# Kernel tuning notes

Measured on AMD Instinct MI355X. Metric: run time of the kernel, lower is better.

The kernel has to match this reference:

```python
import jax, jax.numpy as jnp
import numpy as np

D_INP = 36
D_MODEL = 144              # 4*d_inp so d_ob == 4 (required by increase_dim view: d_ob*8 == 32)
D_OB = D_MODEL // D_INP    # 4
D_PE = 16
MAX_LEN = 215
NHEAD = 4
NHID = 256
NLAYERS = 2
B = 8
L = MAX_LEN
C = MAX_LEN * D_OB         # 860: ob-propagation node feature width
E = D_INP * D_INP          # dense sensor graph incl. self loops
K = E // 2                 # edges kept after pruning (use_beta path)
D_TR = D_MODEL + D_PE      # 160: transformer width


def _layernorm(x, w, b, eps=1e-5):
    mu = x.mean(-1, keepdims=True)
    var = ((x - mu) ** 2).mean(-1, keepdims=True)
    return (x - mu) * jax.lax.rsqrt(var + eps) * w + b


def _pos_encode(times):
    # times [L,B] -> sinusoidal PE [L,B,16] (PositionalEncodingTF)
    ts = jnp.asarray(MAX_LEN ** np.linspace(0.0, 1.0, D_PE // 2), jnp.float32)
    scaled = times[..., None] / ts
    return jnp.concatenate([jnp.sin(scaled), jnp.cos(scaled)], axis=-1)


def _graph_prop(x, p_t, src, dst, ew, W_inc, b_inc, map_w):
    # Two stacked Observation_progation layers for ONE sample.
    # x [N,C] sensor features, p_t [L,16], edges src->dst, edge weights ew [E].
    x_i = x[dst]                                            # target node feats per edge
    x_j = x[src]                                            # source node feats per edge
    hW = (x_i @ W_inc.T + b_inc).reshape(E, L, 32)          # increase_dim + view
    # beta = mean(h_W * cat([map_w[dst] bcast, p_t bcast], -1), -1), computed without materializing aa
    beta = (jnp.einsum('ets,es->et', hW[..., :D_PE], map_w[dst]) +
            jnp.einsum('ets,ts->et', hW[..., D_PE:], p_t)) / 32.0
    gamma = jnp.repeat(beta * ew[:, None], D_OB, axis=-1)   # [E,C]
    top = jnp.argsort(-gamma.mean(axis=1))[:K]              # prune half of the edges
    gamma_p = gamma[top]
    src_p = src[top]
    dst_p = dst[top]
    alpha = gamma_p.mean(axis=-1)                           # layer-1 attention weights [K]
    msg1 = jax.nn.relu(x_j[top]) * jax.nn.relu(gamma_p)
    h1 = jax.ops.segment_sum(msg1, dst_p, num_segments=D_INP)
    # layer 2: use_beta=False, edge_weights = alpha, same pruned edge set
    msg2 = jax.nn.relu(h1[src_p]) * jax.nn.relu(alpha)[:, None]
    h2 = jax.ops.segment_sum(msg2, dst_p, num_segments=D_INP)
    return h2, alpha


def _encoder_layer(x, pad_mask, qkv_w, qkv_b, out_w, out_b,
                   ff1_w, ff1_b, ff2_w, ff2_b, ln1_w, ln1_b, ln2_w, ln2_b):
    # torch post-norm TransformerEncoderLayer (relu, eval mode); x [B,L,D]
    Bq, Lq, D = x.shape
    dh = D // NHEAD
    q, k, v = jnp.split(x @ qkv_w.T + qkv_b, 3, axis=-1)
    hd = lambda t: t.reshape(Bq, Lq, NHEAD, dh).transpose(0, 2, 1, 3)
    scores = jnp.einsum('bhqd,bhkd->bhqk', hd(q), hd(k)) / jnp.sqrt(jnp.float32(dh))
    scores = jnp.where(pad_mask[:, None, None, :], -1e9, scores)  # src_key_padding_mask
    ctx = jnp.einsum('bhqk,bhkd->bhqd', jax.nn.softmax(scores, axis=-1), hd(v))
    ctx = ctx.transpose(0, 2, 1, 3).reshape(Bq, Lq, D)
    x = _layernorm(x + ctx @ out_w.T + out_b, ln1_w, ln1_b)
    ff = jax.nn.relu(x @ ff1_w.T + ff1_b) @ ff2_w.T + ff2_b
    return _layernorm(x + ff, ln2_w, ln2_b)


def _forward(event_type, event_time, R_u, global_structure,
             ob1_W_inc, ob1_b_inc, ob1_map_w, layer_params, w_time, w_type):
    non_pad = (event_type != 0).astype(jnp.float32)[..., None]      # [B,L,1]
    lengths = non_pad[..., 0].sum(axis=-1).astype(jnp.int32)        # [B]
    times = event_time.T                                            # [L,B]
    idx = jnp.maximum(event_type - 1, 0)
    src = jax.nn.one_hot(idx, D_INP, dtype=jnp.float32)             # [B,L,N]
    src = jnp.repeat(jnp.transpose(src, (1, 0, 2)), D_OB, axis=-1)  # [L,B,N*d_ob]
    h = jax.nn.relu(src * R_u[0])                                   # relu(src * R_u)
    pe = _pos_encode(times)                                         # [L,B,16]
    pad_mask = jnp.arange(L)[None, :] >= lengths[:, None]           # [B,L]

    eye = jnp.eye(D_INP, dtype=jnp.float32)
    adj = global_structure * (1.0 - eye) + eye                      # diagonal set to 1
    src_e = jnp.repeat(jnp.arange(D_INP), D_INP)                    # edge_index[0] (row-major nonzero)
    dst_e = jnp.tile(jnp.arange(D_INP), D_INP)                      # edge_index[1]
    ew = adj.reshape(-1)

    def per_sample(xu, pu):  # xu [L,144], pu [L,16]
        sd = xu.reshape(L, D_INP, D_OB).transpose(1, 0, 2).reshape(D_INP, C)
        h2, alpha = _graph_prop(sd, pu, src_e, dst_e, ew, ob1_W_inc, ob1_b_inc, ob1_map_w)
        return h2.reshape(D_INP, L, D_OB).transpose(1, 0, 2).reshape(L, D_INP * D_OB), alpha

    gout, alpha_all = jax.vmap(per_sample, in_axes=(1, 1), out_axes=(1, 1))(h, pe)
    A = alpha_all.T                                                 # [B,K]
    d2 = jnp.sum((A[:, None, :] - A[None, :, :]) ** 2, axis=-1)
    distance = jnp.mean(jnp.where(d2 > 0, jnp.sqrt(jnp.where(d2 > 0, d2, 1.0)), 0.0))

    x = jnp.transpose(jnp.concatenate([gout, pe], axis=2), (1, 0, 2))  # [B,L,160]
    for p in layer_params:
        x = _encoder_layer(x, pad_mask, *p)
    output = x                                                      # == transpose(r_out, 0, 1)
    time_pred = (output @ w_time.T) * non_pad
    type_pred = (output @ w_type.T) * non_pad
    return output, type_pred, time_pred, distance


def setup_inputs():
    key = jax.random.key(0)
    kit = iter(jax.random.split(key, 40))
    def nrm(shape, s=0.05):
        return jax.random.normal(next(kit), shape, dtype=jnp.float32) * s
    lengths = jax.random.randint(next(kit), (B,), 100, L + 1)
    et = jax.random.randint(next(kit), (B, L), 1, D_INP + 1)
    pad = jnp.arange(L)[None, :] >= lengths[:, None]
    inp = {
        'event_type': jnp.where(pad, 0, et).astype(jnp.int32),
        'event_time': jnp.cumsum(jax.random.uniform(next(kit), (B, L)), axis=1).astype(jnp.float32),
        'R_u': nrm((1, D_INP * D_OB), 0.2),
        'global_structure': jax.random.uniform(next(kit), (D_INP, D_INP), minval=0.5, maxval=1.5, dtype=jnp.float32),
        'ob1_W_inc': nrm((C * 8, C), 0.02),
        'ob1_b_inc': jnp.zeros((C * 8,), jnp.float32),
        'ob1_map_w': nrm((D_INP, D_PE), 0.2),
        'w_time': nrm((1, D_TR)),
        'w_type': nrm((D_INP, D_TR)),
    }
    for i in range(NLAYERS):
        inp[f'l{i}_qkv_w'] = nrm((3 * D_TR, D_TR))
        inp[f'l{i}_qkv_b'] = jnp.zeros((3 * D_TR,), jnp.float32)
        inp[f'l{i}_out_w'] = nrm((D_TR, D_TR))
        inp[f'l{i}_out_b'] = jnp.zeros((D_TR,), jnp.float32)
        inp[f'l{i}_ff1_w'] = nrm((NHID, D_TR))
        inp[f'l{i}_ff1_b'] = jnp.zeros((NHID,), jnp.float32)
        inp[f'l{i}_ff2_w'] = nrm((D_TR, NHID))
        inp[f'l{i}_ff2_b'] = jnp.zeros((D_TR,), jnp.float32)
        inp[f'l{i}_ln1_w'] = jnp.ones((D_TR,), jnp.float32)
        inp[f'l{i}_ln1_b'] = jnp.zeros((D_TR,), jnp.float32)
        inp[f'l{i}_ln2_w'] = jnp.ones((D_TR,), jnp.float32)
        inp[f'l{i}_ln2_b'] = jnp.zeros((D_TR,), jnp.float32)
    return inp


def reference(event_type, event_time, R_u, global_structure, ob1_W_inc, ob1_b_inc, ob1_map_w,
              l0_qkv_w, l0_qkv_b, l0_out_w, l0_out_b, l0_ff1_w, l0_ff1_b, l0_ff2_w, l0_ff2_b,
              l0_ln1_w, l0_ln1_b, l0_ln2_w, l0_ln2_b,
              l1_qkv_w, l1_qkv_b, l1_out_w, l1_out_b, l1_ff1_w, l1_ff1_b, l1_ff2_w, l1_ff2_b,
              l1_ln1_w, l1_ln1_b, l1_ln2_w, l1_ln2_b, w_time, w_type):
    lp = [
        (l0_qkv_w, l0_qkv_b, l0_out_w, l0_out_b, l0_ff1_w, l0_ff1_b, l0_ff2_w, l0_ff2_b,
         l0_ln1_w, l0_ln1_b, l0_ln2_w, l0_ln2_b),
        (l1_qkv_w, l1_qkv_b, l1_out_w, l1_out_b, l1_ff1_w, l1_ff1_b, l1_ff2_w, l1_ff2_b,
         l1_ln1_w, l1_ln1_b, l1_ln2_w, l1_ln2_b),
    ]
    return _forward(event_type, event_time, R_u, global_structure,
                    ob1_W_inc, ob1_b_inc, ob1_map_w, lp, w_time, w_type)
```

## Files before the change

kernel.cpp:

```cpp
#include <hip/hip_runtime.h>
#include <math.h>

#define NBATCH 8
#define LMAX   215
#define NND    36
#define NE     1296
#define NK     648
#define CW     860
#define DPE    16
#define DTR    160
#define NHEADS 4
#define DH     40
#define NHID2  256
#define NPAIR  (NBATCH*LMAX)
#define KSPLIT 8
#define KQLEN  27
#define ROWS   4

#define OUT_TYPE (NBATCH*LMAX*DTR)
#define OUT_TIME (OUT_TYPE + NBATCH*LMAX*NND)
#define OUT_DIST (OUT_TIME + NBATCH*LMAX)

#define OFF_PE    0
#define OFF_RR    (OFF_PE + NBATCH*LMAX*DPE)
#define OFF_EW    (OFF_RR + 144)
#define OFF_BETA  (OFF_EW + NE)
#define OFF_ALPHA (OFF_BETA + NBATCH*NND*LMAX)
#define OFF_H1    (OFF_ALPHA + NBATCH*NK)
#define OFF_X     (OFF_H1 + NBATCH*NND*CW)
#define OFF_X2    (OFF_X + NBATCH*LMAX*DTR)
#define OFF_QKV   (OFF_X2 + NBATCH*LMAX*DTR)
#define OFF_TOPI  (OFF_QKV + NBATCH*LMAX*480)
#define OFF_IDX   (OFF_TOPI + NBATCH*NK)
#define OFF_LENS  (OFF_IDX + NBATCH*LMAX)
#define OFF_PART  (OFF_LENS + NBATCH)
#define OFF_CSRC  (OFF_PART + 32*KSPLIT*LMAX*42)
#define OFF_CSRL  (OFF_CSRC + NBATCH*NND)
#define OFF_WT    (OFF_CSRL + NBATCH*NND*LMAX)

__global__ __launch_bounds__(256) void k_wt(
        const float* __restrict__ q0, const float* __restrict__ o0,
        const float* __restrict__ f10, const float* __restrict__ f20,
        const float* __restrict__ q1, const float* __restrict__ o1,
        const float* __restrict__ f11, const float* __restrict__ f21,
        float* __restrict__ wt) {
    int mat = blockIdx.y;
    const float* src; float* dst; int R, C;
    switch (mat) {
        case 0: src = q0;  dst = wt + 0;               R = 480; C = DTR;   break;
        case 1: src = o0;  dst = wt + 76800;           R = DTR; C = DTR;   break;
        case 2: src = f10; dst = wt + 102400;          R = NHID2; C = DTR; break;
        case 3: src = f20; dst = wt + 143360;          R = DTR; C = NHID2; break;
        case 4: src = q1;  dst = wt + 184320;          R = 480; C = DTR;   break;
        case 5: src = o1;  dst = wt + 184320 + 76800;  R = DTR; C = DTR;   break;
        case 6: src = f11; dst = wt + 184320 + 102400; R = NHID2; C = DTR; break;
        default: src = f21; dst = wt + 184320 + 143360; R = DTR; C = NHID2; break;
    }
    int total = R * C;
    for (int i = blockIdx.x * 256 + threadIdx.x; i < total; i += gridDim.x * 256) {
        int r = i / C, c = i - r * C;
        dst[c * R + r] = src[i];
    }
}

__global__ __launch_bounds__(256) void k_prep(
        const int* __restrict__ et, const float* __restrict__ etime,
        const float* __restrict__ Ru, const float* __restrict__ gs,
        float* pe, float* rr, float* ew, int* idxarr, int* lens,
        int* csr_cnt, int* csr_list, float* __restrict__ x) {
    int blk = blockIdx.x, tid = threadIdx.x;
    if (blk == 0) {
        for (int c = tid; c < 144; c += 256) rr[c] = fmaxf(Ru[c], 0.f);
        for (int e = tid; e < NE; e += 256) {
            int r = e / NND, cc = e % NND;
            ew[e] = (r == cc) ? 1.0f : gs[e];
        }
    } else if (blk <= 8) {
        int b = blk - 1;
        __shared__ int red[256];
        __shared__ int sidx[LMAX];
        int cnt = 0;
        for (int l = tid; l < LMAX; l += 256) {
            int v = et[b * LMAX + l];
            cnt += (v != 0);
            int ix = max(v - 1, 0);
            idxarr[b * LMAX + l] = ix;
            sidx[l] = ix;
        }
        red[tid] = cnt;
        __syncthreads();
        for (int st = 128; st > 0; st >>= 1) { if (tid < st) red[tid] += red[tid + st]; __syncthreads(); }
        if (tid == 0) lens[b] = red[0];
        if (tid < NND) {
            int c = 0;
            int* lst = csr_list + (size_t)(b * NND + tid) * LMAX;
            for (int l = 0; l < LMAX; ++l)
                if (sidx[l] == tid) { lst[c] = l; ++c; }
            csr_cnt[b * NND + tid] = c;
        }
    } else {
        __shared__ float sts[8];
        if (tid < 8) sts[tid] = (float)pow(215.0, (double)tid / 7.0);
        __syncthreads();
        int i0 = (blk - 9) * 430;
        for (int i = i0 + tid; i < i0 + 430; i += 256) {
            int s = i & 15; int bl = i >> 4;
            float t = etime[bl];
            float sc = t / sts[s & 7];
            float v = (s < 8) ? sinf(sc) : cosf(sc);
            pe[i] = v;
            x[(size_t)bl * DTR + 144 + s] = v;
        }
    }
}

__global__ __launch_bounds__(256) void k_beta(
        const float* __restrict__ Winc, const float* __restrict__ binc,
        const float* __restrict__ mapw, const float* __restrict__ pe,
        const float* __restrict__ rr, const int* __restrict__ idxarr,
        const int* __restrict__ csr_cnt, const int* __restrict__ csr_list,
        float* __restrict__ beta) {
    const int t = blockIdx.x;
    const int tid = threadIdx.x;

    __shared__ float s_rows[2][4 * CW];
    __shared__ float s_pair[NBATCH * LMAX];
    __shared__ int   s_idx[NPAIR];
    __shared__ float s_mapw[NND * 16];
    __shared__ float s_rr[144];
    __shared__ float s_pe[NBATCH * 16];
    __shared__ float s_binc[32];

    for (int i = tid; i < NPAIR; i += 256) s_idx[i] = idxarr[i];
    for (int i = tid; i < NND * 16; i += 256) s_mapw[i] = mapw[i];
    if (tid < 144) s_rr[tid] = rr[tid];
    if (tid < 128) { int b = tid >> 4, s = tid & 15; s_pe[tid] = pe[((size_t)(b * LMAX + t)) * DPE + s]; }
    if (tid < 32) s_binc[tid] = binc[32 * t + tid];

    float4 pre[4];
    {
        const float4* src = (const float4*)(Winc + (size_t)(32 * t) * CW);
#pragma unroll
        for (int i = 0; i < 4; ++i) { int k = tid + i * 256; if (k < CW) pre[i] = src[k]; }
    }
    __syncthreads();

    const int l = tid;
    int nb[NBATCH];
    float4 r4b[NBATCH];
    if (l < LMAX) {
#pragma unroll
        for (int b = 0; b < NBATCH; ++b) {
            nb[b] = s_idx[b * LMAX + l];
            r4b[b] = *(const float4*)&s_rr[4 * nb[b]];
        }
    }
    float acc[NBATCH];
#pragma unroll
    for (int b = 0; b < NBATCH; ++b) acc[b] = 0.f;

    int p = 0;
    for (int jc = 0; jc < 8; ++jc) {
        float4* buf = (float4*)&s_rows[p][0];
#pragma unroll
        for (int i = 0; i < 4; ++i) { int k = tid + i * 256; if (k < CW) buf[k] = pre[i]; }
        __syncthreads();
        if (jc < 7) {
            const float4* src = (const float4*)(Winc + (size_t)(32 * t + 4 * (jc + 1)) * CW);
#pragma unroll
            for (int i = 0; i < 4; ++i) { int k = tid + i * 256; if (k < CW) pre[i] = src[k]; }
        }
        if (l < LMAX) {
            if (jc < 4) {
#pragma unroll
                for (int jj = 0; jj < 4; ++jj) {
                    int j = 4 * jc + jj;
                    float4 w4 = *(const float4*)&s_rows[p][jj * CW + 4 * l];
#pragma unroll
                    for (int b = 0; b < NBATCH; ++b) {
                        float dv = r4b[b].x * w4.x + r4b[b].y * w4.y + r4b[b].z * w4.z + r4b[b].w * w4.w;
                        acc[b] += s_mapw[nb[b] * 16 + j] * dv;
                    }
                }
            } else {
#pragma unroll
                for (int jj = 0; jj < 4; ++jj) {
                    int j = 4 * jc + jj;
                    float4 w4 = *(const float4*)&s_rows[p][jj * CW + 4 * l];
#pragma unroll
                    for (int b = 0; b < NBATCH; ++b) {
                        float dv = r4b[b].x * w4.x + r4b[b].y * w4.y + r4b[b].z * w4.z + r4b[b].w * w4.w;
                        acc[b] += s_pe[(b << 4) + (j - 16)] * dv;
                    }
                }
            }
        }
        __syncthreads();
        p ^= 1;
    }

    if (l < LMAX) {
#pragma unroll
        for (int b = 0; b < NBATCH; ++b) s_pair[b * LMAX + l] = acc[b];
    }
    __syncthreads();

    for (int bn = tid; bn < NBATCH * NND; bn += 256) {
        int b = bn / NND, n = bn - b * NND;
        int cnt = csr_cnt[bn];
        const int* lst = csr_list + (size_t)bn * LMAX;
        float sum = 0.f;
        for (int i = 0; i < cnt; ++i) sum += s_pair[b * LMAX + lst[i]];
        float bias = 0.f;
#pragma unroll
        for (int s = 0; s < 16; ++s)
            bias += s_mapw[n * 16 + s] * s_binc[s] + s_pe[(b << 4) + s] * s_binc[16 + s];
        beta[(size_t)bn * LMAX + t] = (sum + bias) * (1.0f / 32.0f);
    }
}

__global__ __launch_bounds__(256) void k_topk(const float* __restrict__ ew,
                                              const float* __restrict__ beta,
                                              int* __restrict__ topi, float* __restrict__ alpha) {
    int chunk = blockIdx.x;
    int b = blockIdx.y;
    int tid = threadIdx.x;
    __shared__ float sv[NE];
    __shared__ float sm[NND];
    int wv = tid >> 6, lane = tid & 63;
    for (int n = wv; n < NND; n += 4) {
        const float* p = beta + (size_t)(b * NND + n) * LMAX;
        float s = 0.f;
        for (int t = lane; t < LMAX; t += 64) s += p[t];
        for (int off = 32; off > 0; off >>= 1) s += __shfl_xor(s, off);
        if (lane == 0) sm[n] = s / (float)LMAX;
    }
    __syncthreads();
    for (int e = tid; e < NE; e += 256) sv[e] = ew[e] * sm[e % NND];
    __syncthreads();
    int e = chunk * 216 + tid;
    if (tid < 216) {
        float v = sv[e];
        int rank = 0;
        for (int i = 0; i < NE; ++i) {
            float u = sv[i];
            rank += (u > v) || (u == v && i < e);
        }
        if (rank < NK) {
            topi[b * NK + rank] = e;
            alpha[b * NK + rank] = v;
        }
    }
}

__global__ void k_h1(const int* __restrict__ topi, const float* __restrict__ ew,
                     const float* __restrict__ beta, const int* __restrict__ idxarr,
                     const float* __restrict__ rr, const float* __restrict__ alpha,
                     float* h1, float* __restrict__ outd) {
    int b = blockIdx.x / NND, n = blockIdx.x % NND;
    __shared__ int cnt;
    __shared__ int lsrc[40];
    __shared__ float lew[40];
    int tid = threadIdx.x;
    if (tid == 0) cnt = 0;
    __syncthreads();
    for (int k = tid; k < NK; k += 256) {
        int e = topi[b * NK + k];
        if (e % NND == n) {
            int p = atomicAdd(&cnt, 1);
            lsrc[p] = e / NND;
            lew[p] = ew[e];
        }
    }
    __syncthreads();
    int m = cnt;
    const float* bb = beta + ((size_t)b * NND + n) * LMAX;
    for (int c = tid; c < CW; c += 256) {
        int t = c >> 2, o = c & 3;
        float bt = bb[t];
        int id = idxarr[b * LMAX + t];
        float x = rr[id * 4 + o];
        float acc = 0.f;
        for (int j = 0; j < m; ++j) {
            float g = bt * lew[j];
            if (g > 0.f && lsrc[j] == id) acc += x * g;
        }
        h1[((size_t)b * NND + n) * CW + c] = acc;
    }
    if (blockIdx.x == 0) {
        __shared__ float sd[64];
        if (tid < 64) {
            int i = tid / 8, j = tid % 8;
            float d2 = 0.f;
            for (int k = 0; k < NK; ++k) {
                float d = alpha[i * NK + k] - alpha[j * NK + k];
                d2 += d * d;
            }
            sd[tid] = (d2 > 0.f) ? sqrtf(d2) : 0.f;
        }
        __syncthreads();
        for (int st = 32; st > 0; st >>= 1) { if (tid < st) sd[tid] += sd[tid + st]; __syncthreads(); }
        if (tid == 0) *outd = sd[0] / 64.0f;
    }
}

__global__ void k_h2(const int* __restrict__ topi, const float* __restrict__ alpha,
                     const float* __restrict__ h1, float* __restrict__ x) {
    int b = blockIdx.x / NND, n = blockIdx.x % NND;
    __shared__ int cnt;
    __shared__ int lsrc[40];
    __shared__ float lal[40];
    int tid = threadIdx.x;
    if (tid == 0) cnt = 0;
    __syncthreads();
    for (int k = tid; k < NK; k += 256) {
        int e = topi[b * NK + k];
        if (e % NND == n) {
            int p = atomicAdd(&cnt, 1);
            lsrc[p] = e / NND;
            lal[p] = fmaxf(alpha[b * NK + k], 0.f);
        }
    }
    __syncthreads();
    int m = cnt;
    for (int c = tid; c < CW; c += 256) {
        float acc = 0.f;
        for (int j = 0; j < m; ++j)
            acc += fmaxf(h1[((size_t)b * NND + lsrc[j]) * CW + c], 0.f) * lal[j];
        x[(size_t)(b * LMAX + (c >> 2)) * DTR + 4 * n + (c & 3)] = acc;
    }
}

__global__ __launch_bounds__(256) void k_qkv(const float* __restrict__ X, const float* __restrict__ WT,
                                             const float* __restrict__ bias, float* __restrict__ Y) {
    int m0 = blockIdx.x * ROWS;
    int tid = threadIdx.x;
    __shared__ float xs[ROWS * DTR];
    for (int i = tid; i < ROWS * DTR; i += 256) xs[i] = X[(size_t)m0 * DTR + i];
    __syncthreads();
    for (int n = tid; n < 480; n += 256) {
        float a[ROWS][4];
#pragma unroll
        for (int r = 0; r < ROWS; ++r) { a[r][0] = a[r][1] = a[r][2] = a[r][3] = 0.f; }
        for (int d = 0; d < DTR; d += 4) {
            float w0 = WT[(size_t)(d + 0) * 480 + n];
            float w1 = WT[(size_t)(d + 1) * 480 + n];
            float w2 = WT[(size_t)(d + 2) * 480 + n];
            float w3 = WT[(size_t)(d + 3) * 480 + n];
#pragma unroll
            for (int r = 0; r < ROWS; ++r) {
                a[r][0] += xs[r * DTR + d] * w0;
                a[r][1] += xs[r * DTR + d + 1] * w1;
                a[r][2] += xs[r * DTR + d + 2] * w2;
                a[r][3] += xs[r * DTR + d + 3] * w3;
            }
        }
        float bv = bias[n];
#pragma unroll
        for (int r = 0; r < ROWS; ++r)
            Y[(size_t)(m0 + r) * 480 + n] = bv + (a[r][0] + a[r][1]) + (a[r][2] + a[r][3]);
    }
}

__global__ __launch_bounds__(256) void k_attn_part(const float* __restrict__ qkv,
                                                   const int* __restrict__ lens,
                                                   float* __restrict__ part) {
    int kq = blockIdx.x;
    int bh = blockIdx.y;
    int b = bh >> 2, h = bh & 3;
    int tid = threadIdx.x;
    int k0 = kq * KQLEN;
    int k1 = min(LMAX, k0 + KQLEN);
    int klen = max(k1 - k0, 0);
    __shared__ float sK[KQLEN * DH];
    __shared__ float sV[KQLEN * DH];
    for (int i = tid; i < klen * DH; i += 256) {
        int kk = i / DH, d = i - kk * DH;
        size_t base = (size_t)(b * LMAX + k0 + kk) * 480;
        sK[i] = qkv[base + DTR + h * DH + d];
        sV[i] = qkv[base + 2 * DTR + h * DH + d];
    }
    __syncthreads();
    int q = tid;
    if (q >= LMAX) return;
    float4 qv[10];
    const float4* qr = (const float4*)(qkv + (size_t)(b * LMAX + q) * 480 + h * DH);
#pragma unroll
    for (int i = 0; i < 10; ++i) qv[i] = qr[i];
    int len = lens[b];
    const float scale = 0.15811388300841898f;
    float m = -INFINITY, l = 0.f;
    float o[DH];
#pragma unroll
    for (int d = 0; d < DH; ++d) o[d] = 0.f;
    int kend = min(k1, len);
    for (int k = k0; k < kend; ++k) {
        const float4* kr = (const float4*)&sK[(k - k0) * DH];
        float s0 = 0.f, s1 = 0.f, s2 = 0.f, s3 = 0.f;
#pragma unroll
        for (int i = 0; i < 10; ++i) {
            float4 kv = kr[i];
            s0 += qv[i].x * kv.x; s1 += qv[i].y * kv.y;
            s2 += qv[i].z * kv.z; s3 += qv[i].w * kv.w;
        }
        float s = ((s0 + s1) + (s2 + s3)) * scale;
        float p;
        if (s <= m) {
            p = expf(s - m);
        } else {
            float c = expf(m - s);
#pragma unroll
            for (int d = 0; d < DH; ++d) o[d] *= c;
            l *= c;
            m = s;
            p = 1.0f;
        }
        l += p;
        const float* vr = &sV[(k - k0) * DH];
#pragma unroll
        for (int d = 0; d < DH; ++d) o[d] += p * vr[d];
    }
    float* pp = part + ((size_t)(bh * KSPLIT + kq) * LMAX + q) * 42;
#pragma unroll
    for (int d = 0; d < DH; ++d) pp[d] = o[d];
    pp[40] = l;
    pp[41] = m;
}

__device__ __forceinline__ void wave_ln_row(const float* __restrict__ row, int lane,
                                            const float* __restrict__ lnw, const float* __restrict__ lnb,
                                            float* __restrict__ dst) {
    float s = 0.f;
    for (int d = lane; d < DTR; d += 64) s += row[d];
    for (int off = 32; off > 0; off >>= 1) s += __shfl_xor(s, off);
    float mu = s / (float)DTR;
    float v = 0.f;
    for (int d = lane; d < DTR; d += 64) { float dd = row[d] - mu; v += dd * dd; }
    for (int off = 32; off > 0; off >>= 1) v += __shfl_xor(v, off);
    float rs = rsqrtf(v / (float)DTR + 1e-5f);
    for (int d = lane; d < DTR; d += 64)
        dst[d] = (row[d] - mu) * rs * lnw[d] + lnb[d];
}

__global__ __launch_bounds__(256) void k_projln(const float* __restrict__ part, const float* __restrict__ xres,
                                                const float* __restrict__ WT, const float* __restrict__ bias,
                                                const float* __restrict__ lnw, const float* __restrict__ lnb,
                                                float* __restrict__ out) {
    int m0 = blockIdx.x * ROWS;
    int tid = threadIdx.x;
    __shared__ float xs[ROWS * DTR];
    __shared__ float ys[ROWS * DTR];
    int g = tid >> 6, lane = tid & 63;
    for (int pr = g; pr < ROWS * NHEADS; pr += 4) {
        int r = pr >> 2, h = pr & 3;
        int row = m0 + r;
        int b = row / LMAX, q = row - b * LMAX;
        const float* pb = part + ((size_t)((b * NHEADS + h) * KSPLIT) * LMAX + q) * 42;
        const size_t st = (size_t)LMAX * 42;
        float ms = -INFINITY;
#pragma unroll
        for (int i = 0; i < KSPLIT; ++i) ms = fmaxf(ms, pb[i * st + 41]);
        float lsum = 0.f, acc = 0.f;
#pragma unroll
        for (int i = 0; i < KSPLIT; ++i) {
            float w = expf(pb[i * st + 41] - ms);
            lsum += w * pb[i * st + 40];
            if (lane < DH) acc += w * pb[i * st + lane];
        }
        if (lane < DH) xs[r * DTR + h * DH + lane] = acc / lsum;
    }
    __syncthreads();
    if (tid < DTR) {
        int n = tid;
        float a[ROWS][4];
#pragma unroll
        for (int r = 0; r < ROWS; ++r) { a[r][0] = a[r][1] = a[r][2] = a[r][3] = 0.f; }
        for (int d = 0; d < DTR; d += 4) {
            float w0 = WT[(size_t)(d + 0) * DTR + n];
            float w1 = WT[(size_t)(d + 1) * DTR + n];
            float w2 = WT[(size_t)(d + 2) * DTR + n];
            float w3 = WT[(size_t)(d + 3) * DTR + n];
#pragma unroll
            for (int r = 0; r < ROWS; ++r) {
                a[r][0] += xs[r * DTR + d] * w0;
                a[r][1] += xs[r * DTR + d + 1] * w1;
                a[r][2] += xs[r * DTR + d + 2] * w2;
                a[r][3] += xs[r * DTR + d + 3] * w3;
            }
        }
        float bv = bias[n];
#pragma unroll
        for (int r = 0; r < ROWS; ++r)
            ys[r * DTR + n] = bv + (a[r][0] + a[r][1]) + (a[r][2] + a[r][3])
                              + xres[(size_t)(m0 + r) * DTR + n];
    }
    __syncthreads();
    if (g < ROWS)
        wave_ln_row(&ys[g * DTR], lane, lnw, lnb, out + (size_t)(m0 + g) * DTR);
}

__global__ __launch_bounds__(256) void k_ffln(const float* __restrict__ xin,
                                              const float* __restrict__ W1T, const float* __restrict__ b1,
                                              const float* __restrict__ W2T, const float* __restrict__ b2,
                                              const float* __restrict__ lnw, const float* __restrict__ lnb,
                                              float* __restrict__ out, int last,
                                              const float* __restrict__ wty, const float* __restrict__ wti,
                                              const int* __restrict__ lens) {
    int m0 = blockIdx.x * ROWS;
    int tid = threadIdx.x;
    __shared__ float xs[ROWS * DTR];
    __shared__ float hs[ROWS * NHID2];
    __shared__ float zs[ROWS * DTR];
    __shared__ float fin[ROWS * DTR];
    for (int i = tid; i < ROWS * DTR; i += 256) xs[i] = xin[(size_t)m0 * DTR + i];
    __syncthreads();
    {
        int n = tid;
        float a[ROWS][4];
#pragma unroll
        for (int r = 0; r < ROWS; ++r) { a[r][0] = a[r][1] = a[r][2] = a[r][3] = 0.f; }
        for (int d = 0; d < DTR; d += 4) {
            float w0 = W1T[(size_t)(d + 0) * NHID2 + n];
            float w1 = W1T[(size_t)(d + 1) * NHID2 + n];
            float w2 = W1T[(size_t)(d + 2) * NHID2 + n];
            float w3 = W1T[(size_t)(d + 3) * NHID2 + n];
#pragma unroll
            for (int r = 0; r < ROWS; ++r) {
                a[r][0] += xs[r * DTR + d] * w0;
                a[r][1] += xs[r * DTR + d + 1] * w1;
                a[r][2] += xs[r * DTR + d + 2] * w2;
                a[r][3] += xs[r * DTR + d + 3] * w3;
            }
        }
        float bv = b1[n];
#pragma unroll
        for (int r = 0; r < ROWS; ++r)
            hs[r * NHID2 + n] = fmaxf(bv + (a[r][0] + a[r][1]) + (a[r][2] + a[r][3]), 0.f);
    }
    __syncthreads();
    if (tid < DTR) {
        int n = tid;
        float a[ROWS][4];
#pragma unroll
        for (int r = 0; r < ROWS; ++r) { a[r][0] = a[r][1] = a[r][2] = a[r][3] = 0.f; }
        for (int d = 0; d < NHID2; d += 4) {
            float w0 = W2T[(size_t)(d + 0) * DTR + n];
            float w1 = W2T[(size_t)(d + 1) * DTR + n];
            float w2 = W2T[(size_t)(d + 2) * DTR + n];
            float w3 = W2T[(size_t)(d + 3) * DTR + n];
#pragma unroll
            for (int r = 0; r < ROWS; ++r) {
                a[r][0] += hs[r * NHID2 + d] * w0;
                a[r][1] += hs[r * NHID2 + d + 1] * w1;
                a[r][2] += hs[r * NHID2 + d + 2] * w2;
                a[r][3] += hs[r * NHID2 + d + 3] * w3;
            }
        }
        float bv = b2[n];
#pragma unroll
        for (int r = 0; r < ROWS; ++r)
            zs[r * DTR + n] = bv + (a[r][0] + a[r][1]) + (a[r][2] + a[r][3]) + xs[r * DTR + n];
    }
    __syncthreads();
    int wid = tid >> 6, lane = tid & 63;
    if (!last) {
        if (wid < ROWS)
            wave_ln_row(&zs[wid * DTR], lane, lnw, lnb, out + (size_t)(m0 + wid) * DTR);
        return;
    }
    if (wid < ROWS)
        wave_ln_row(&zs[wid * DTR], lane, lnw, lnb, &fin[wid * DTR]);
    __syncthreads();
    for (int i = tid; i < ROWS * DTR; i += 256) out[(size_t)m0 * DTR + i] = fin[i];
    {
        int row = m0 + wid;
        int b = row / LMAX, l = row - b * LMAX;
        float np = (l < lens[b]) ? 1.f : 0.f;
        if (lane < 37) {
            const float* w = (lane < 36) ? (wty + lane * DTR) : wti;
            const float* fr = &fin[wid * DTR];
            float acc = 0.f;
#pragma unroll 8
            for (int d = 0; d < DTR; d += 4) {
                float4 w4 = *(const float4*)(w + d);
                acc += fr[d] * w4.x + fr[d + 1] * w4.y + fr[d + 2] * w4.z + fr[d + 3] * w4.w;
            }
            acc *= np;
            if (lane < 36) out[OUT_TYPE + (size_t)row * NND + lane] = acc;
            else out[OUT_TIME + row] = acc;
        }
    }
}

extern "C" void kernel_launch(void* const* d_in, const int* in_sizes, int n_in,
                              void* d_out, int out_size, void* d_ws, size_t ws_size,
                              hipStream_t stream) {
    const int* et      = (const int*)d_in[0];
    const float* etime = (const float*)d_in[1];
    const float* Ru    = (const float*)d_in[2];
    const float* gs    = (const float*)d_in[3];
    const float* Winc  = (const float*)d_in[4];
    const float* binc  = (const float*)d_in[5];
    const float* mapw  = (const float*)d_in[6];
    const float* wtime = (const float*)d_in[7];
    const float* wtype = (const float*)d_in[8];

    float* ws   = (float*)d_ws;
    float* pe   = ws + OFF_PE;
    float* rr   = ws + OFF_RR;
    float* ew   = ws + OFF_EW;
    float* beta = ws + OFF_BETA;
    float* alpha= ws + OFF_ALPHA;
    float* h1   = ws + OFF_H1;
    float* x    = ws + OFF_X;
    float* x2   = ws + OFF_X2;
    float* qkvb = ws + OFF_QKV;
    float* part = ws + OFF_PART;
    float* wt   = ws + OFF_WT;
    int* topi   = (int*)(ws + OFF_TOPI);
    int* idxarr = (int*)(ws + OFF_IDX);
    int* lens   = (int*)(ws + OFF_LENS);
    int* csrc   = (int*)(ws + OFF_CSRC);
    int* csrl   = (int*)(ws + OFF_CSRL);
    float* outp = (float*)d_out;

    k_wt<<<dim3(32, 8), 256, 0, stream>>>(
        (const float*)d_in[9],  (const float*)d_in[11], (const float*)d_in[13], (const float*)d_in[15],
        (const float*)d_in[21], (const float*)d_in[23], (const float*)d_in[25], (const float*)d_in[27], wt);
    k_prep<<<73, 256, 0, stream>>>(et, etime, Ru, gs, pe, rr, ew, idxarr, lens, csrc, csrl, x);
    k_beta<<<LMAX, 256, 0, stream>>>(Winc, binc, mapw, pe, rr, idxarr, csrc, csrl, beta);
    k_topk<<<dim3(6, NBATCH), 256, 0, stream>>>(ew, beta, topi, alpha);
    k_h1<<<NBATCH * NND, 256, 0, stream>>>(topi, ew, beta, idxarr, rr, alpha, h1, outp + OUT_DIST);
    k_h2<<<NBATCH * NND, 256, 0, stream>>>(topi, alpha, h1, x);

    const int MB4 = NPAIR / ROWS;
    for (int layer = 0; layer < 2; ++layer) {
        int base = 9 + layer * 12;
        const float* qkv_b = (const float*)d_in[base + 1];
        const float* out_b = (const float*)d_in[base + 3];
        const float* ff1_b = (const float*)d_in[base + 5];
        const float* ff2_b = (const float*)d_in[base + 7];
        const float* ln1_w = (const float*)d_in[base + 8];
        const float* ln1_b = (const float*)d_in[base + 9];
        const float* ln2_w = (const float*)d_in[base + 10];
        const float* ln2_b = (const float*)d_in[base + 11];
        const float* qkvT = wt + (size_t)layer * 184320;
        const float* outT = qkvT + 76800;
        const float* ff1T = qkvT + 102400;
        const float* ff2T = qkvT + 143360;

        k_qkv<<<MB4, 256, 0, stream>>>(x, qkvT, qkv_b, qkvb);
        k_attn_part<<<dim3(KSPLIT, NBATCH * NHEADS), 256, 0, stream>>>(qkvb, lens, part);
        k_projln<<<MB4, 256, 0, stream>>>(part, x, outT, out_b, ln1_w, ln1_b, x2);
        if (layer == 0)
            k_ffln<<<MB4, 256, 0, stream>>>(x2, ff1T, ff1_b, ff2T, ff2_b, ln2_w, ln2_b,
                                            x, 0, wtype, wtime, lens);
        else
            k_ffln<<<MB4, 256, 0, stream>>>(x2, ff1T, ff1_b, ff2T, ff2_b, ln2_w, ln2_b,
                                            outp, 1, wtype, wtime, lens);
    }
}
```

Baseline: 419.3 us.

## Fuse all stages into one persistent megakernel with software grid barriers

Result: slower. 750.5 us (+79.0%).

```diff
diff --git a/kernel.cpp b/kernel.cpp
--- a/kernel.cpp
+++ b/kernel.cpp
@@ -16,6 +16,8 @@
 #define KSPLIT 8
 #define KQLEN  27
 #define ROWS   4
+#define NBLK   430
+#define MAGIC  0x5A5A5A5A
 
 #define OUT_TYPE (NBATCH*LMAX*DTR)
 #define OUT_TIME (OUT_TYPE + NBATCH*LMAX*NND)
@@ -37,399 +39,49 @@
 #define OFF_CSRC  (OFF_PART + 32*KSPLIT*LMAX*42)
 #define OFF_CSRL  (OFF_CSRC + NBATCH*NND)
 #define OFF_WT    (OFF_CSRL + NBATCH*NND*LMAX)
-
-__global__ __launch_bounds__(256) void k_wt(
-        const float* __restrict__ q0, const float* __restrict__ o0,
-        const float* __restrict__ f10, const float* __restrict__ f20,
-        const float* __restrict__ q1, const float* __restrict__ o1,
-        const float* __restrict__ f11, const float* __restrict__ f21,
-        float* __restrict__ wt) {
-    int mat = blockIdx.y;
-    const float* src; float* dst; int R, C;
-    switch (mat) {
-        case 0: src = q0;  dst = wt + 0;               R = 480; C = DTR;   break;
-        case 1: src = o0;  dst = wt + 76800;           R = DTR; C = DTR;   break;
-        case 2: src = f10; dst = wt + 102400;          R = NHID2; C = DTR; break;
-        case 3: src = f20; dst = wt + 143360;          R = DTR; C = NHID2; break;
-        case 4: src = q1;  dst = wt + 184320;          R = 480; C = DTR;   break;
-        case 5: src = o1;  dst = wt + 184320 + 76800;  R = DTR; C = DTR;   break;
-        case 6: src = f11; dst = wt + 184320 + 102400; R = NHID2; C = DTR; break;
-        default: src = f21; dst = wt + 184320 + 143360; R = DTR; C = NHID2; break;
-    }
-    int total = R * C;
-    for (int i = blockIdx.x * 256 + threadIdx.x; i < total; i += gridDim.x * 256) {
-        int r = i / C, c = i - r * C;
-        dst[c * R + r] = src[i];
-    }
+#define OFF_BAR   (OFF_WT + 2*184320)
+
+struct MegaArgs {
+    const int* et; const float* etime; const float* Ru; const float* gs;
+    const float* Winc; const float* binc; const float* mapw;
+    const float* wtime; const float* wtype;
+    const float* qw[2];  const float* qb[2];
+    const float* ow[2];  const float* ob[2];
+    const float* f1w[2]; const float* f1b[2];
+    const float* f2w[2]; const float* f2b[2];
+    const float* l1w[2]; const float* l1b[2];
+    const float* l2w[2]; const float* l2b[2];
+    float* ws; float* outp;
+};
+
+struct SBeta { float rows[2][4*CW]; float pair[NPAIR]; int idx[NPAIR];
+               float mapw[NND*16]; float rr[144]; float pe[NBATCH*16]; float binc[32]; };
+struct SPrep { int red[256]; int sidx[LMAX]; float sts[8]; };
+struct STopk { float sv[NE]; float sm[NND]; };
+struct SAttn { float K[KQLEN*DH]; float V[KQLEN*DH]; };
+struct SH1   { int cnt; int lsrc[40]; float lew[40]; float sd[64]; };
+struct SH2   { int cnt; int lsrc[40]; float lal[40]; };
+struct SQkv  { float xs[ROWS*DTR]; };
+struct SProj { float xs[ROWS*DTR]; float ys[ROWS*DTR]; };
+struct SFf   { float xs[ROWS*DTR]; float hs[ROWS*NHID2]; float zs[ROWS*DTR]; float fin[ROWS*DTR]; };
+
+__device__ __forceinline__ void gridbar(int* cnt, int* gen, int bi) {
+    __syncthreads();
+    if (threadIdx.x == 0) {
+        int old = __hip_atomic_fetch_add(&cnt[bi], 1, __ATOMIC_ACQ_REL, __HIP_MEMORY_SCOPE_AGENT);
+        if (old == NBLK - 1) {
+            __hip_atomic_store(gen, bi + 1, __ATOMIC_RELEASE, __HIP_MEMORY_SCOPE_AGENT);
+        } else {
+            while (__hip_atomic_load(gen, __ATOMIC_RELAXED, __HIP_MEMORY_SCOPE_AGENT) < bi + 1)
+                __builtin_amdgcn_s_sleep(2);
+            (void)__hip_atomic_load(gen, __ATOMIC_ACQUIRE, __HIP_MEMORY_SCOPE_AGENT);
+        }
+    }
+    __syncthreads();
 }
 
-__global__ __launch_bounds__(256) void k_prep(
-        const int* __restrict__ et, const float* __restrict__ etime,
-        const float* __restrict__ Ru, const float* __restrict__ gs,
-        float* pe, float* rr, float* ew, int* idxarr, int* lens,
-        int* csr_cnt, int* csr_list, float* __restrict__ x) {
-    int blk = blockIdx.x, tid = threadIdx.x;
-    if (blk == 0) {
-        for (int c = tid; c < 144; c += 256) rr[c] = fmaxf(Ru[c], 0.f);
-        for (int e = tid; e < NE; e += 256) {
-            int r = e / NND, cc = e % NND;
-            ew[e] = (r == cc) ? 1.0f : gs[e];
-        }
-    } else if (blk <= 8) {
-        int b = blk - 1;
-        __shared__ int red[256];
-        __shared__ int sidx[LMAX];
-        int cnt = 0;
-        for (int l = tid; l < LMAX; l += 256) {
-            int v = et[b * LMAX + l];
-            cnt += (v != 0);
-            int ix = max(v - 1, 0);
-            idxarr[b * LMAX + l] = ix;
-            sidx[l] = ix;
-        }
-        red[tid] = cnt;
-        __syncthreads();
-        for (int st = 128; st > 0; st >>= 1) { if (tid < st) red[tid] += red[tid + st]; __syncthreads(); }
-        if (tid == 0) lens[b] = red[0];
-        if (tid < NND) {
-            int c = 0;
-            int* lst = csr_list + (size_t)(b * NND + tid) * LMAX;
-            for (int l = 0; l < LMAX; ++l)
-                if (sidx[l] == tid) { lst[c] = l; ++c; }
-            csr_cnt[b * NND + tid] = c;
-        }
-    } else {
-        __shared__ float sts[8];
-        if (tid < 8) sts[tid] = (float)pow(215.0, (double)tid / 7.0);
-        __syncthreads();
-        int i0 = (blk - 9) * 430;
-        for (int i = i0 + tid; i < i0 + 430; i += 256) {
-            int s = i & 15; int bl = i >> 4;
-            float t = etime[bl];
-            float sc = t / sts[s & 7];
-            float v = (s < 8) ? sinf(sc) : cosf(sc);
-            pe[i] = v;
-            x[(size_t)bl * DTR + 144 + s] = v;
-        }
-    }
-}
-
-__global__ __launch_bounds__(256) void k_beta(
-        const float* __restrict__ Winc, const float* __restrict__ binc,
-        const float* __restrict__ mapw, const float* __restrict__ pe,
-        const float* __restrict__ rr, const int* __restrict__ idxarr,
-        const int* __restrict__ csr_cnt, const int* __restrict__ csr_list,
-        float* __restrict__ beta) {
-    const int t = blockIdx.x;
-    const int tid = threadIdx.x;
-
-    __shared__ float s_rows[2][4 * CW];
-    __shared__ float s_pair[NBATCH * LMAX];
-    __shared__ int   s_idx[NPAIR];
-    __shared__ float s_mapw[NND * 16];
-    __shared__ float s_rr[144];
-    __shared__ float s_pe[NBATCH * 16];
-    __shared__ float s_binc[32];
-
-    for (int i = tid; i < NPAIR; i += 256) s_idx[i] = idxarr[i];
-    for (int i = tid; i < NND * 16; i += 256) s_mapw[i] = mapw[i];
-    if (tid < 144) s_rr[tid] = rr[tid];
-    if (tid < 128) { int b = tid >> 4, s = tid & 15; s_pe[tid] = pe[((size_t)(b * LMAX + t)) * DPE + s]; }
-    if (tid < 32) s_binc[tid] = binc[32 * t + tid];
-
-    float4 pre[4];
-    {
-        const float4* src = (const float4*)(Winc + (size_t)(32 * t) * CW);
-#pragma unroll
-        for (int i = 0; i < 4; ++i) { int k = tid + i * 256; if (k < CW) pre[i] = src[k]; }
-    }
-    __syncthreads();
-
-    const int l = tid;
-    int nb[NBATCH];
-    float4 r4b[NBATCH];
-    if (l < LMAX) {
-#pragma unroll
-        for (int b = 0; b < NBATCH; ++b) {
-            nb[b] = s_idx[b * LMAX + l];
-            r4b[b] = *(const float4*)&s_rr[4 * nb[b]];
-        }
-    }
-    float acc[NBATCH];
-#pragma unroll
-    for (int b = 0; b < NBATCH; ++b) acc[b] = 0.f;
-
-    int p = 0;
-    for (int jc = 0; jc < 8; ++jc) {
-        float4* buf = (float4*)&s_rows[p][0];
-#pragma unroll
-        for (int i = 0; i < 4; ++i) { int k = tid + i * 256; if (k < CW) buf[k] = pre[i]; }
-        __syncthreads();
-        if (jc < 7) {
-            const float4* src = (const float4*)(Winc + (size_t)(32 * t + 4 * (jc + 1)) * CW);
-#pragma unroll
-            for (int i = 0; i < 4; ++i) { int k = tid + i * 256; if (k < CW) pre[i] = src[k]; }
-        }
-        if (l < LMAX) {
-            if (jc < 4) {
-#pragma unroll
-                for (int jj = 0; jj < 4; ++jj) {
-                    int j = 4 * jc + jj;
-                    float4 w4 = *(const float4*)&s_rows[p][jj * CW + 4 * l];
-#pragma unroll
-                    for (int b = 0; b < NBATCH; ++b) {
-                        float dv = r4b[b].x * w4.x + r4b[b].y * w4.y + r4b[b].z * w4.z + r4b[b].w * w4.w;
-                        acc[b] += s_mapw[nb[b] * 16 + j] * dv;
-                    }
-                }
-            } else {
-#pragma unroll
-                for (int jj = 0; jj < 4; ++jj) {
-                    int j = 4 * jc + jj;
-                    float4 w4 = *(const float4*)&s_rows[p][jj * CW + 4 * l];
-#pragma unroll
-                    for (int b = 0; b < NBATCH; ++b) {
-                        float dv = r4b[b].x * w4.x + r4b[b].y * w4.y + r4b[b].z * w4.z + r4b[b].w * w4.w;
-                        acc[b] += s_pe[(b << 4) + (j - 16)] * dv;
-                    }
-                }
-            }
-        }
-        __syncthreads();
-        p ^= 1;
-    }
-
-    if (l < LMAX) {
-#pragma unroll
-        for (int b = 0; b < NBATCH; ++b) s_pair[b * LMAX + l] = acc[b];
-    }
-    __syncthreads();
-
-    for (int bn = tid; bn < NBATCH * NND; bn += 256) {
-        int b = bn / NND, n = bn - b * NND;
-        int cnt = csr_cnt[bn];
-        const int* lst = csr_list + (size_t)bn * LMAX;
-        float sum = 0.f;
-        for (int i = 0; i < cnt; ++i) sum += s_pair[b * LMAX + lst[i]];
-        float bias = 0.f;
-#pragma unroll
-        for (int s = 0; s < 16; ++s)
-            bias += s_mapw[n * 16 + s] * s_binc[s] + s_pe[(b << 4) + s] * s_binc[16 + s];
-        beta[(size_t)bn * LMAX + t] = (sum + bias) * (1.0f / 32.0f);
-    }
-}
-
-__global__ __launch_bounds__(256) void k_topk(const float* __restrict__ ew,
-                                              const float* __restrict__ beta,
-                                              int* __restrict__ topi, float* __restrict__ alpha) {
-    int chunk = blockIdx.x;
-    int b = blockIdx.y;
-    int tid = threadIdx.x;
-    __shared__ float sv[NE];
-    __shared__ float sm[NND];
-    int wv = tid >> 6, lane = tid & 63;
-    for (int n = wv; n < NND; n += 4) {
-        const float* p = beta + (size_t)(b * NND + n) * LMAX;
-        float s = 0.f;
-        for (int t = lane; t < LMAX; t += 64) s += p[t];
-        for (int off = 32; off > 0; off >>= 1) s += __shfl_xor(s, off);
-        if (lane == 0) sm[n] = s / (float)LMAX;
-    }
-    __syncthreads();
-    for (int e = tid; e < NE; e += 256) sv[e] = ew[e] * sm[e % NND];
-    __syncthreads();
-    int e = chunk * 216 + tid;
-    if (tid < 216) {
-        float v = sv[e];
-        int rank = 0;
-        for (int i = 0; i < NE; ++i) {
-            float u = sv[i];
-            rank += (u > v) || (u == v && i < e);
-        }
-        if (rank < NK) {
-            topi[b * NK + rank] = e;
-            alpha[b * NK + rank] = v;
-        }
-    }
-}
-
-__global__ void k_h1(const int* __restrict__ topi, const float* __restrict__ ew,
-                     const float* __restrict__ beta, const int* __restrict__ idxarr,
-                     const float* __restrict__ rr, const float* __restrict__ alpha,
-                     float* h1, float* __restrict__ outd) {
-    int b = blockIdx.x / NND, n = blockIdx.x % NND;
-    __shared__ int cnt;
-    __shared__ int lsrc[40];
-    __shared__ float lew[40];
-    int tid = threadIdx.x;
-    if (tid == 0) cnt = 0;
-    __syncthreads();
-    for (int k = tid; k < NK; k += 256) {
-        int e = topi[b * NK + k];
-        if (e % NND == n) {
-            int p = atomicAdd(&cnt, 1);
-            lsrc[p] = e / NND;
-            lew[p] = ew[e];
-        }
-    }
-    __syncthreads();
-    int m = cnt;
-    const float* bb = beta + ((size_t)b * NND + n) * LMAX;
-    for (int c = tid; c < CW; c += 256) {
-        int t = c >> 2, o = c & 3;
-        float bt = bb[t];
-        int id = idxarr[b * LMAX + t];
-        float x = rr[id * 4 + o];
-        float acc = 0.f;
-        for (int j = 0; j < m; ++j) {
-            float g = bt * lew[j];
-            if (g > 0.f && lsrc[j] == id) acc += x * g;
-        }
-        h1[((size_t)b * NND + n) * CW + c] = acc;
-    }
-    if (blockIdx.x == 0) {
-        __shared__ float sd[64];
-        if (tid < 64) {
-            int i = tid / 8, j = tid % 8;
-            float d2 = 0.f;
-            for (int k = 0; k < NK; ++k) {
-                float d = alpha[i * NK + k] - alpha[j * NK + k];
-                d2 += d * d;
-            }
-            sd[tid] = (d2 > 0.f) ? sqrtf(d2) : 0.f;
-        }
-        __syncthreads();
-        for (int st = 32; st > 0; st >>= 1) { if (tid < st) sd[tid] += sd[tid + st]; __syncthreads(); }
-        if (tid == 0) *outd = sd[0] / 64.0f;
-    }
-}
-
-__global__ void k_h2(const int* __restrict__ topi, const float* __restrict__ alpha,
-                     const float* __restrict__ h1, float* __restrict__ x) {
-    int b = blockIdx.x / NND, n = blockIdx.x % NND;
-    __shared__ int cnt;
-    __shared__ int lsrc[40];
-    __shared__ float lal[40];
-    int tid = threadIdx.x;
-    if (tid == 0) cnt = 0;
-    __syncthreads();
-    for (int k = tid; k < NK; k += 256) {
-        int e = topi[b * NK + k];
-        if (e % NND == n) {
-            int p = atomicAdd(&cnt, 1);
-            lsrc[p] = e / NND;
-            lal[p] = fmaxf(alpha[b * NK + k], 0.f);
-        }
-    }
-    __syncthreads();
-    int m = cnt;
-    for (int c = tid; c < CW; c += 256) {
-        float acc = 0.f;
-        for (int j = 0; j < m; ++j)
-            acc += fmaxf(h1[((size_t)b * NND + lsrc[j]) * CW + c], 0.f) * lal[j];
-        x[(size_t)(b * LMAX + (c >> 2)) * DTR + 4 * n + (c & 3)] = acc;
-    }
-}
-
-__global__ __launch_bounds__(256) void k_qkv(const float* __restrict__ X, const float* __restrict__ WT,
-                                             const float* __restrict__ bias, float* __restrict__ Y) {
-    int m0 = blockIdx.x * ROWS;
-    int tid = threadIdx.x;
-    __shared__ float xs[ROWS * DTR];
-    for (int i = tid; i < ROWS * DTR; i += 256) xs[i] = X[(size_t)m0 * DTR + i];
-    __syncthreads();
-    for (int n = tid; n < 480; n += 256) {
-        float a[ROWS][4];
-#pragma unroll
-        for (int r = 0; r < ROWS; ++r) { a[r][0] = a[r][1] = a[r][2] = a[r][3] = 0.f; }
-        for (int d = 0; d < DTR; d += 4) {
-            float w0 = WT[(size_t)(d + 0) * 480 + n];
-            float w1 = WT[(size_t)(d + 1) * 480 + n];
-            float w2 = WT[(size_t)(d + 2) * 480 + n];
-            float w3 = WT[(size_t)(d + 3) * 480 + n];
-#pragma unroll
-            for (int r = 0; r < ROWS; ++r) {
-                a[r][0] += xs[r * DTR + d] * w0;
-                a[r][1] += xs[r * DTR + d + 1] * w1;
-                a[r][2] += xs[r * DTR + d + 2] * w2;
-                a[r][3] += xs[r * DTR + d + 3] * w3;
-            }
-        }
-        float bv = bias[n];
-#pragma unroll
-        for (int r = 0; r < ROWS; ++r)
-            Y[(size_t)(m0 + r) * 480 + n] = bv + (a[r][0] + a[r][1]) + (a[r][2] + a[r][3]);
-    }
-}
-
-__global__ __launch_bounds__(256) void k_attn_part(const float* __restrict__ qkv,
-                                                   const int* __restrict__ lens,
-                                                   float* __restrict__ part) {
-    int kq = blockIdx.x;
-    int bh = blockIdx.y;
-    int b = bh >> 2, h = bh & 3;
-    int tid = threadIdx.x;
-    int k0 = kq * KQLEN;
-    int k1 = min(LMAX, k0 + KQLEN);
-    int klen = max(k1 - k0, 0);
-    __shared__ float sK[KQLEN * DH];
-    __shared__ float sV[KQLEN * DH];
-    for (int i = tid; i < klen * DH; i += 256) {
-        int kk = i / DH, d = i - kk * DH;
-        size_t base = (size_t)(b * LMAX + k0 + kk) * 480;
-        sK[i] = qkv[base + DTR + h * DH + d];
-        sV[i] = qkv[base + 2 * DTR + h * DH + d];
-    }
-    __syncthreads();
-    int q = tid;
-    if (q >= LMAX) return;
-    float4 qv[10];
-    const float4* qr = (const float4*)(qkv + (size_t)(b * LMAX + q) * 480 + h * DH);
-#pragma unroll
-    for (int i = 0; i < 10; ++i) qv[i] = qr[i];
-    int len = lens[b];
-    const float scale = 0.15811388300841898f;
-    float m = -INFINITY, l = 0.f;
-    float o[DH];
-#pragma unroll
-    for (int d = 0; d < DH; ++d) o[d] = 0.f;
-    int kend = min(k1, len);
-    for (int k = k0; k < kend; ++k) {
-        const float4* kr = (const float4*)&sK[(k - k0) * DH];
-        float s0 = 0.f, s1 = 0.f, s2 = 0.f, s3 = 0.f;
-#pragma unroll
-        for (int i = 0; i < 10; ++i) {
-            float4 kv = kr[i];
-            s0 += qv[i].x * kv.x; s1 += qv[i].y * kv.y;
-            s2 += qv[i].z * kv.z; s3 += qv[i].w * kv.w;
-        }
-        float s = ((s0 + s1) + (s2 + s3)) * scale;
-        float p;
-        if (s <= m) {
-            p = expf(s - m);
-        } else {
-            float c = expf(m - s);
-#pragma unroll
-            for (int d = 0; d < DH; ++d) o[d] *= c;
-            l *= c;
-            m = s;
-            p = 1.0f;
-        }
-        l += p;
-        const float* vr = &sV[(k - k0) * DH];
-#pragma unroll
-        for (int d = 0; d < DH; ++d) o[d] += p * vr[d];
-    }
-    float* pp = part + ((size_t)(bh * KSPLIT + kq) * LMAX + q) * 42;
-#pragma unroll
-    for (int d = 0; d < DH; ++d) pp[d] = o[d];
-    pp[40] = l;
-    pp[41] = m;
-}
-
-__device__ __forceinline__ void wave_ln_row(const float* __restrict__ row, int lane,
-                                            const float* __restrict__ lnw, const float* __restrict__ lnb,
-                                            float* __restrict__ dst) {
+__device__ __forceinline__ void wave_ln_row(const float* row, int lane,
+                                            const float* lnw, const float* lnb, float* dst) {
     float s = 0.f;
     for (int d = lane; d < DTR; d += 64) s += row[d];
     for (int off = 32; off > 0; off >>= 1) s += __shfl_xor(s, off);
@@ -442,221 +94,570 @@
         dst[d] = (row[d] - mu) * rs * lnw[d] + lnb[d];
 }
 
-__global__ __launch_bounds__(256) void k_projln(const float* __restrict__ part, const float* __restrict__ xres,
-                                                const float* __restrict__ WT, const float* __restrict__ bias,
-                                                const float* __restrict__ lnw, const float* __restrict__ lnb,
-                                                float* __restrict__ out) {
-    int m0 = blockIdx.x * ROWS;
-    int tid = threadIdx.x;
-    __shared__ float xs[ROWS * DTR];
-    __shared__ float ys[ROWS * DTR];
-    int g = tid >> 6, lane = tid & 63;
-    for (int pr = g; pr < ROWS * NHEADS; pr += 4) {
-        int r = pr >> 2, h = pr & 3;
-        int row = m0 + r;
-        int b = row / LMAX, q = row - b * LMAX;
-        const float* pb = part + ((size_t)((b * NHEADS + h) * KSPLIT) * LMAX + q) * 42;
-        const size_t st = (size_t)LMAX * 42;
-        float ms = -INFINITY;
-#pragma unroll
-        for (int i = 0; i < KSPLIT; ++i) ms = fmaxf(ms, pb[i * st + 41]);
-        float lsum = 0.f, acc = 0.f;
-#pragma unroll
-        for (int i = 0; i < KSPLIT; ++i) {
-            float w = expf(pb[i * st + 41] - ms);
-            lsum += w * pb[i * st + 40];
-            if (lane < DH) acc += w * pb[i * st + lane];
-        }
-        if (lane < DH) xs[r * DTR + h * DH + lane] = acc / lsum;
-    }
-    __syncthreads();
-    if (tid < DTR) {
-        int n = tid;
-        float a[ROWS][4];
-#pragma unroll
-        for (int r = 0; r < ROWS; ++r) { a[r][0] = a[r][1] = a[r][2] = a[r][3] = 0.f; }
-        for (int d = 0; d < DTR; d += 4) {
-            float w0 = WT[(size_t)(d + 0) * DTR + n];
-            float w1 = WT[(size_t)(d + 1) * DTR + n];
-            float w2 = WT[(size_t)(d + 2) * DTR + n];
-            float w3 = WT[(size_t)(d + 3) * DTR + n];
-#pragma unroll
-            for (int r = 0; r < ROWS; ++r) {
-                a[r][0] += xs[r * DTR + d] * w0;
-                a[r][1] += xs[r * DTR + d + 1] * w1;
-                a[r][2] += xs[r * DTR + d + 2] * w2;
-                a[r][3] += xs[r * DTR + d + 3] * w3;
-            }
-        }
-        float bv = bias[n];
-#pragma unroll
-        for (int r = 0; r < ROWS; ++r)
-            ys[r * DTR + n] = bv + (a[r][0] + a[r][1]) + (a[r][2] + a[r][3])
-                              + xres[(size_t)(m0 + r) * DTR + n];
-    }
-    __syncthreads();
-    if (g < ROWS)
-        wave_ln_row(&ys[g * DTR], lane, lnw, lnb, out + (size_t)(m0 + g) * DTR);
-}
-
-__global__ __launch_bounds__(256) void k_ffln(const float* __restrict__ xin,
-                                              const float* __restrict__ W1T, const float* __restrict__ b1,
-                                              const float* __restrict__ W2T, const float* __restrict__ b2,
-                                              const float* __restrict__ lnw, const float* __restrict__ lnb,
-                                              float* __restrict__ out, int last,
-                                              const float* __restrict__ wty, const float* __restrict__ wti,
-                                              const int* __restrict__ lens) {
-    int m0 = blockIdx.x * ROWS;
-    int tid = threadIdx.x;
-    __shared__ float xs[ROWS * DTR];
-    __shared__ float hs[ROWS * NHID2];
-    __shared__ float zs[ROWS * DTR];
-    __shared__ float fin[ROWS * DTR];
-    for (int i = tid; i < ROWS * DTR; i += 256) xs[i] = xin[(size_t)m0 * DTR + i];
-    __syncthreads();
-    {
-        int n = tid;
-        float a[ROWS][4];
-#pragma unroll
-        for (int r = 0; r < ROWS; ++r) { a[r][0] = a[r][1] = a[r][2] = a[r][3] = 0.f; }
-        for (int d = 0; d < DTR; d += 4) {
-            float w0 = W1T[(size_t)(d + 0) * NHID2 + n];
-            float w1 = W1T[(size_t)(d + 1) * NHID2 + n];
-            float w2 = W1T[(size_t)(d + 2) * NHID2 + n];
-            float w3 = W1T[(size_t)(d + 3) * NHID2 + n];
-#pragma unroll
-            for (int r = 0; r < ROWS; ++r) {
-                a[r][0] += xs[r * DTR + d] * w0;
-                a[r][1] += xs[r * DTR + d + 1] * w1;
-                a[r][2] += xs[r * DTR + d + 2] * w2;
-                a[r][3] += xs[r * DTR + d + 3] * w3;
-            }
-        }
-        float bv = b1[n];
-#pragma unroll
-        for (int r = 0; r < ROWS; ++r)
-            hs[r * NHID2 + n] = fmaxf(bv + (a[r][0] + a[r][1]) + (a[r][2] + a[r][3]), 0.f);
-    }
-    __syncthreads();
-    if (tid < DTR) {
-        int n = tid;
-        float a[ROWS][4];
-#pragma unroll
-        for (int r = 0; r < ROWS; ++r) { a[r][0] = a[r][1] = a[r][2] = a[r][3] = 0.f; }
-        for (int d = 0; d < NHID2; d += 4) {
-            float w0 = W2T[(size_t)(d + 0) * DTR + n];
-            float w1 = W2T[(size_t)(d + 1) * DTR + n];
-            float w2 = W2T[(size_t)(d + 2) * DTR + n];
-            float w3 = W2T[(size_t)(d + 3) * DTR + n];
-#pragma unroll
-            for (int r = 0; r < ROWS; ++r) {
-                a[r][0] += hs[r * NHID2 + d] * w0;
-                a[r][1] += hs[r * NHID2 + d + 1] * w1;
-                a[r][2] += hs[r * NHID2 + d + 2] * w2;
-                a[r][3] += hs[r * NHID2 + d + 3] * w3;
-            }
-        }
-        float bv = b2[n];
-#pragma unroll
-        for (int r = 0; r < ROWS; ++r)
-            zs[r * DTR + n] = bv + (a[r][0] + a[r][1]) + (a[r][2] + a[r][3]) + xs[r * DTR + n];
-    }
-    __syncthreads();
-    int wid = tid >> 6, lane = tid & 63;
-    if (!last) {
-        if (wid < ROWS)
-            wave_ln_row(&zs[wid * DTR], lane, lnw, lnb, out + (size_t)(m0 + wid) * DTR);
-        return;
-    }
-    if (wid < ROWS)
-        wave_ln_row(&zs[wid * DTR], lane, lnw, lnb, &fin[wid * DTR]);
-    __syncthreads();
-    for (int i = tid; i < ROWS * DTR; i += 256) out[(size_t)m0 * DTR + i] = fin[i];
-    {
-        int row = m0 + wid;
-        int b = row / LMAX, l = row - b * LMAX;
-        float np = (l < lens[b]) ? 1.f : 0.f;
-        if (lane < 37) {
-            const float* w = (lane < 36) ? (wty + lane * DTR) : wti;
-            const float* fr = &fin[wid * DTR];
-            float acc = 0.f;
-#pragma unroll 8
-            for (int d = 0; d < DTR; d += 4) {
-                float4 w4 = *(const float4*)(w + d);
-                acc += fr[d] * w4.x + fr[d + 1] * w4.y + fr[d + 2] * w4.z + fr[d + 3] * w4.w;
-            }
-            acc *= np;
-            if (lane < 36) out[OUT_TYPE + (size_t)row * NND + lane] = acc;
-            else out[OUT_TIME + row] = acc;
-        }
-    }
-}
-
-extern "C" void kernel_launch(void* const* d_in, const int* in_sizes, int n_in,
-                              void* d_out, int out_size, void* d_ws, size_t ws_size,
-                              hipStream_t stream) {
-    const int* et      = (const int*)d_in[0];
-    const float* etime = (const float*)d_in[1];
-    const float* Ru    = (const float*)d_in[2];
-    const float* gs    = (const float*)d_in[3];
-    const float* Winc  = (const float*)d_in[4];
-    const float* binc  = (const float*)d_in[5];
-    const float* mapw  = (const float*)d_in[6];
-    const float* wtime = (const float*)d_in[7];
-    const float* wtype = (const float*)d_in[8];
-
-    float* ws   = (float*)d_ws;
-    float* pe   = ws + OFF_PE;
-    float* rr   = ws + OFF_RR;
-    float* ew   = ws + OFF_EW;
-    float* beta = ws + OFF_BETA;
-    float* alpha= ws + OFF_ALPHA;
-    float* h1   = ws + OFF_H1;
-    float* x    = ws + OFF_X;
-    float* x2   = ws + OFF_X2;
-    float* qkvb = ws + OFF_QKV;
-    float* part = ws + OFF_PART;
-    float* wt   = ws + OFF_WT;
+__global__ __launch_bounds__(256, 2) void k_mega(MegaArgs a) {
+    __shared__ __align__(16) char smem[45056];
+    const int wb = blockIdx.x;
+    const int tid = threadIdx.x;
+
+    float* ws = a.ws;
+    float* pe    = ws + OFF_PE;
+    float* rr    = ws + OFF_RR;
+    float* ew    = ws + OFF_EW;
+    float* beta  = ws + OFF_BETA;
+    float* alpha = ws + OFF_ALPHA;
+    float* h1    = ws + OFF_H1;
+    float* x     = ws + OFF_X;
+    float* x2    = ws + OFF_X2;
+    float* qkvb  = ws + OFF_QKV;
+    float* part  = ws + OFF_PART;
+    float* wt    = ws + OFF_WT;
     int* topi   = (int*)(ws + OFF_TOPI);
     int* idxarr = (int*)(ws + OFF_IDX);
     int* lens   = (int*)(ws + OFF_LENS);
     int* csrc   = (int*)(ws + OFF_CSRC);
     int* csrl   = (int*)(ws + OFF_CSRL);
-    float* outp = (float*)d_out;
-
-    k_wt<<<dim3(32, 8), 256, 0, stream>>>(
-        (const float*)d_in[9],  (const float*)d_in[11], (const float*)d_in[13], (const float*)d_in[15],
-        (const float*)d_in[21], (const float*)d_in[23], (const float*)d_in[25], (const float*)d_in[27], wt);
-    k_prep<<<73, 256, 0, stream>>>(et, etime, Ru, gs, pe, rr, ew, idxarr, lens, csrc, csrl, x);
-    k_beta<<<LMAX, 256, 0, stream>>>(Winc, binc, mapw, pe, rr, idxarr, csrc, csrl, beta);
-    k_topk<<<dim3(6, NBATCH), 256, 0, stream>>>(ew, beta, topi, alpha);
-    k_h1<<<NBATCH * NND, 256, 0, stream>>>(topi, ew, beta, idxarr, rr, alpha, h1, outp + OUT_DIST);
-    k_h2<<<NBATCH * NND, 256, 0, stream>>>(topi, alpha, h1, x);
-
-    const int MB4 = NPAIR / ROWS;
+    int* bar    = (int*)(ws + OFF_BAR);
+    int* gen    = bar + 16;
+    int* ready  = bar + 17;
+    float* outp = a.outp;
+
+    if (wb == 0 && tid == 0) {
+        for (int i = 0; i < 16; ++i)
+            __hip_atomic_store(&bar[i], 0, __ATOMIC_RELAXED, __HIP_MEMORY_SCOPE_AGENT);
+        __hip_atomic_store(gen, 0, __ATOMIC_RELAXED, __HIP_MEMORY_SCOPE_AGENT);
+        __hip_atomic_store(ready, MAGIC, __ATOMIC_RELEASE, __HIP_MEMORY_SCOPE_AGENT);
+    } else if (tid == 0) {
+        while (__hip_atomic_load(ready, __ATOMIC_RELAXED, __HIP_MEMORY_SCOPE_AGENT) != MAGIC)
+            __builtin_amdgcn_s_sleep(2);
+        (void)__hip_atomic_load(ready, __ATOMIC_ACQUIRE, __HIP_MEMORY_SCOPE_AGENT);
+    }
+    __syncthreads();
+
+    if (wb == 0) {
+        for (int c = tid; c < 144; c += 256) rr[c] = fmaxf(a.Ru[c], 0.f);
+        for (int e = tid; e < NE; e += 256) {
+            int r = e / NND, cc = e % NND;
+            ew[e] = (r == cc) ? 1.0f : a.gs[e];
+        }
+    } else if (wb <= 8) {
+        SPrep* sp = (SPrep*)smem;
+        int b = wb - 1;
+        int cnt = 0;
+        for (int l = tid; l < LMAX; l += 256) {
+            int v = a.et[b * LMAX + l];
+            cnt += (v != 0);
+            int ix = max(v - 1, 0);
+            idxarr[b * LMAX + l] = ix;
+            sp->sidx[l] = ix;
+        }
+        sp->red[tid] = cnt;
+        __syncthreads();
+        for (int st = 128; st > 0; st >>= 1) { if (tid < st) sp->red[tid] += sp->red[tid + st]; __syncthreads(); }
+        if (tid == 0) lens[b] = sp->red[0];
+        if (tid < NND) {
+            int c = 0;
+            int* lst = csrl + (size_t)(b * NND + tid) * LMAX;
+            for (int l = 0; l < LMAX; ++l)
+                if (sp->sidx[l] == tid) { lst[c] = l; ++c; }
+            csrc[b * NND + tid] = c;
+        }
+    } else if (wb <= 72) {
+        SPrep* sp = (SPrep*)smem;
+        if (tid < 8) sp->sts[tid] = (float)pow(215.0, (double)tid / 7.0);
+        __syncthreads();
+        int i0 = (wb - 9) * 430;
+        for (int i = i0 + tid; i < i0 + 430; i += 256) {
+            int s = i & 15; int bl = i >> 4;
+            float t = a.etime[bl];
+            float sc = t / sp->sts[s & 7];
+            float v = (s < 8) ? sinf(sc) : cosf(sc);
+            pe[i] = v;
+            x[(size_t)bl * DTR + 144 + s] = v;
+        }
+    } else if (wb < 73 + 256) {
+        int idx = wb - 73;
+        int mat = idx >> 5, sub = idx & 31;
+        const float* src; float* dst; int R, C;
+        switch (mat) {
+            case 0: src = a.qw[0];  dst = wt + 0;               R = 480;   C = DTR;   break;
+            case 1: src = a.ow[0];  dst = wt + 76800;           R = DTR;   C = DTR;   break;
+            case 2: src = a.f1w[0]; dst = wt + 102400;          R = NHID2; C = DTR;   break;
+            case 3: src = a.f2w[0]; dst = wt + 143360;          R = DTR;   C = NHID2; break;
+            case 4: src = a.qw[1];  dst = wt + 184320;          R = 480;   C = DTR;   break;
+            case 5: src = a.ow[1];  dst = wt + 184320 + 76800;  R = DTR;   C = DTR;   break;
+            case 6: src = a.f1w[1]; dst = wt + 184320 + 102400; R = NHID2; C = DTR;   break;
+            default: src = a.f2w[1]; dst = wt + 184320 + 143360; R = DTR;  C = NHID2; break;
+        }
+        int total = R * C;
+        for (int i = sub * 256 + tid; i < total; i += 32 * 256) {
+            int r = i / C, c = i - r * C;
+            dst[c * R + r] = src[i];
+        }
+    }
+    gridbar(bar, gen, 0);
+
+    if (wb < LMAX) {
+        SBeta* sb = (SBeta*)smem;
+        const int t = wb;
+        for (int i = tid; i < NPAIR; i += 256) sb->idx[i] = idxarr[i];
+        for (int i = tid; i < NND * 16; i += 256) sb->mapw[i] = a.mapw[i];
+        if (tid < 144) sb->rr[tid] = rr[tid];
+        if (tid < 128) { int b = tid >> 4, s = tid & 15; sb->pe[tid] = pe[((size_t)(b * LMAX + t)) * DPE + s]; }
+        if (tid < 32) sb->binc[tid] = a.binc[32 * t + tid];
+
+        float4 pre[4];
+        {
+            const float4* src = (const float4*)(a.Winc + (size_t)(32 * t) * CW);
+#pragma unroll
+            for (int i = 0; i < 4; ++i) { int k = tid + i * 256; if (k < CW) pre[i] = src[k]; }
+        }
+        __syncthreads();
+
+        const int l = tid;
+        int nb[NBATCH];
+        float4 r4b[NBATCH];
+        if (l < LMAX) {
+#pragma unroll
+            for (int b = 0; b < NBATCH; ++b) {
+                nb[b] = sb->idx[b * LMAX + l];
+                r4b[b] = *(const float4*)&sb->rr[4 * nb[b]];
+            }
+        }
+        float acc[NBATCH];
+#pragma unroll
+        for (int b = 0; b < NBATCH; ++b) acc[b] = 0.f;
+
+        int p = 0;
+        for (int jc = 0; jc < 8; ++jc) {
+            float4* buf = (float4*)&sb->rows[p][0];
+#pragma unroll
+            for (int i = 0; i < 4; ++i) { int k = tid + i * 256; if (k < CW) buf[k] = pre[i]; }
+            __syncthreads();
+            if (jc < 7) {
+                const float4* src = (const float4*)(a.Winc + (size_t)(32 * t + 4 * (jc + 1)) * CW);
+#pragma unroll
+                for (int i = 0; i < 4; ++i) { int k = tid + i * 256; if (k < CW) pre[i] = src[k]; }
+            }
+            if (l < LMAX) {
+                if (jc < 4) {
+#pragma unroll
+                    for (int jj = 0; jj < 4; ++jj) {
+                        int j = 4 * jc + jj;
+                        float4 w4 = *(const float4*)&sb->rows[p][jj * CW + 4 * l];
+#pragma unroll
+                        for (int b = 0; b < NBATCH; ++b) {
+                            float dv = r4b[b].x * w4.x + r4b[b].y * w4.y + r4b[b].z * w4.z + r4b[b].w * w4.w;
+                            acc[b] += sb->mapw[nb[b] * 16 + j] * dv;
+                        }
+                    }
+                } else {
+#pragma unroll
+                    for (int jj = 0; jj < 4; ++jj) {
+                        int j = 4 * jc + jj;
+                        float4 w4 = *(const float4*)&sb->rows[p][jj * CW + 4 * l];
+#pragma unroll
+                        for (int b = 0; b < NBATCH; ++b) {
+                            float dv = r4b[b].x * w4.x + r4b[b].y * w4.y + r4b[b].z * w4.z + r4b[b].w * w4.w;
+                            acc[b] += sb->pe[(b << 4) + (j - 16)] * dv;
+                        }
+                    }
+                }
+            }
+            __syncthreads();
+            p ^= 1;
+        }
+
+        if (l < LMAX) {
+#pragma unroll
+            for (int b = 0; b < NBATCH; ++b) sb->pair[b * LMAX + l] = acc[b];
+        }
+        __syncthreads();
+
+        for (int bn = tid; bn < NBATCH * NND; bn += 256) {
+            int b = bn / NND, n = bn - b * NND;
+            int cnt = csrc[bn];
+            const int* lst = csrl + (size_t)bn * LMAX;
+            float sum = 0.f;
+            for (int i = 0; i < cnt; ++i) sum += sb->pair[b * LMAX + lst[i]];
+            float bias = 0.f;
+#pragma unroll
+            for (int s = 0; s < 16; ++s)
+                bias += sb->mapw[n * 16 + s] * sb->binc[s] + sb->pe[(b << 4) + s] * sb->binc[16 + s];
+            beta[(size_t)bn * LMAX + t] = (sum + bias) * (1.0f / 32.0f);
+        }
+    }
+    gridbar(bar, gen, 1);
+
+    if (wb < 48) {
+        STopk* st = (STopk*)smem;
+        int chunk = wb % 6, b = wb / 6;
+        int wv = tid >> 6, lane = tid & 63;
+        for (int n = wv; n < NND; n += 4) {
+            const float* p = beta + (size_t)(b * NND + n) * LMAX;
+            float s = 0.f;
+            for (int t = lane; t < LMAX; t += 64) s += p[t];
+            for (int off = 32; off > 0; off >>= 1) s += __shfl_xor(s, off);
+            if (lane == 0) st->sm[n] = s / (float)LMAX;
+        }
+        __syncthreads();
+        for (int e = tid; e < NE; e += 256) st->sv[e] = ew[e] * st->sm[e % NND];
+        __syncthreads();
+        int e = chunk * 216 + tid;
+        if (tid < 216) {
+            float v = st->sv[e];
+            int rank = 0;
+            for (int i = 0; i < NE; ++i) {
+                float u = st->sv[i];
+                rank += (u > v) || (u == v && i < e);
+            }
+            if (rank < NK) {
+                topi[b * NK + rank] = e;
+                alpha[b * NK + rank] = v;
+            }
+        }
+    }
+    gridbar(bar, gen, 2);
+
+    if (wb < NBATCH * NND) {
+        SH1* sh = (SH1*)smem;
+        int b = wb / NND, n = wb % NND;
+        if (tid == 0) sh->cnt = 0;
+        __syncthreads();
+        for (int k = tid; k < NK; k += 256) {
+            int e = topi[b * NK + k];
+            if (e % NND == n) {
+                int p = atomicAdd(&sh->cnt, 1);
+                sh->lsrc[p] = e / NND;
+                sh->lew[p] = ew[e];
+            }
+        }
+        __syncthreads();
+        int m = sh->cnt;
+        const float* bb = beta + ((size_t)b * NND + n) * LMAX;
+        for (int c = tid; c < CW; c += 256) {
+            int t = c >> 2, o = c & 3;
+            float bt = bb[t];
+            int id = idxarr[b * LMAX + t];
+            float xv = rr[id * 4 + o];
+            float acc = 0.f;
+            for (int j = 0; j < m; ++j) {
+                float g = bt * sh->lew[j];
+                if (g > 0.f && sh->lsrc[j] == id) acc += xv * g;
+            }
+            h1[((size_t)b * NND + n) * CW + c] = acc;
+        }
+        if (wb == 0) {
+            if (tid < 64) {
+                int i = tid / 8, j = tid % 8;
+                float d2 = 0.f;
+                for (int k = 0; k < NK; ++k) {
+                    float d = alpha[i * NK + k] - alpha[j * NK + k];
+                    d2 += d * d;
+                }
+                sh->sd[tid] = (d2 > 0.f) ? sqrtf(d2) : 0.f;
+            }
+            __syncthreads();
+            for (int st = 32; st > 0; st >>= 1) { if (tid < st) sh->sd[tid] += sh->sd[tid + st]; __syncthreads(); }
+            if (tid == 0) outp[OUT_DIST] = sh->sd[0] / 64.0f;
+        }
+    }
+    gridbar(bar, gen, 3);
+
+    if (wb < NBATCH * NND) {
+        SH2* sh = (SH2*)smem;
+        int b = wb / NND, n = wb % NND;
+        if (tid == 0) sh->cnt = 0;
+        __syncthreads();
+        for (int k = tid; k < NK; k += 256) {
+            int e = topi[b * NK + k];
+            if (e % NND == n) {
+                int p = atomicAdd(&sh->cnt, 1);
+                sh->lsrc[p] = e / NND;
+                sh->lal[p] = fmaxf(alpha[b * NK + k], 0.f);
+            }
+        }
+        __syncthreads();
+        int m = sh->cnt;
+        for (int c = tid; c < CW; c += 256) {
+            float acc = 0.f;
+            for (int j = 0; j < m; ++j)
+                acc += fmaxf(h1[((size_t)b * NND + sh->lsrc[j]) * CW + c], 0.f) * sh->lal[j];
+            x[(size_t)(b * LMAX + (c >> 2)) * DTR + 4 * n + (c & 3)] = acc;
+        }
+    }
+    gridbar(bar, gen, 4);
+
     for (int layer = 0; layer < 2; ++layer) {
-        int base = 9 + layer * 12;
-        const float* qkv_b = (const float*)d_in[base + 1];
-        const float* out_b = (const float*)d_in[base + 3];
-        const float* ff1_b = (const float*)d_in[base + 5];
-        const float* ff2_b = (const float*)d_in[base + 7];
-        const float* ln1_w = (const float*)d_in[base + 8];
-        const float* ln1_b = (const float*)d_in[base + 9];
-        const float* ln2_w = (const float*)d_in[base + 10];
-        const float* ln2_b = (const float*)d_in[base + 11];
         const float* qkvT = wt + (size_t)layer * 184320;
         const float* outT = qkvT + 76800;
         const float* ff1T = qkvT + 102400;
         const float* ff2T = qkvT + 143360;
-
-        k_qkv<<<MB4, 256, 0, stream>>>(x, qkvT, qkv_b, qkvb);
-        k_attn_part<<<dim3(KSPLIT, NBATCH * NHEADS), 256, 0, stream>>>(qkvb, lens, part);
-        k_projln<<<MB4, 256, 0, stream>>>(part, x, outT, out_b, ln1_w, ln1_b, x2);
-        if (layer == 0)
-            k_ffln<<<MB4, 256, 0, stream>>>(x2, ff1T, ff1_b, ff2T, ff2_b, ln2_w, ln2_b,
-                                            x, 0, wtype, wtime, lens);
-        else
-            k_ffln<<<MB4, 256, 0, stream>>>(x2, ff1T, ff1_b, ff2T, ff2_b, ln2_w, ln2_b,
-                                            outp, 1, wtype, wtime, lens);
+        const float* in_x = x;
+        float* ff_out = (layer == 0) ? x : outp;
+
+        {
+            SQkv* sq = (SQkv*)smem;
+            int m0 = wb * ROWS;
+            for (int i = tid; i < ROWS * DTR; i += 256) sq->xs[i] = in_x[(size_t)m0 * DTR + i];
+            __syncthreads();
+            for (int n = tid; n < 480; n += 256) {
+                float acr[ROWS][4];
+#pragma unroll
+                for (int r = 0; r < ROWS; ++r) { acr[r][0] = acr[r][1] = acr[r][2] = acr[r][3] = 0.f; }
+                for (int d = 0; d < DTR; d += 4) {
+                    float w0 = qkvT[(size_t)(d + 0) * 480 + n];
+                    float w1 = qkvT[(size_t)(d + 1) * 480 + n];
+                    float w2 = qkvT[(size_t)(d + 2) * 480 + n];
+                    float w3 = qkvT[(size_t)(d + 3) * 480 + n];
+#pragma unroll
+                    for (int r = 0; r < ROWS; ++r) {
+                        acr[r][0] += sq->xs[r * DTR + d] * w0;
+                        acr[r][1] += sq->xs[r * DTR + d + 1] * w1;
+                        acr[r][2] += sq->xs[r * DTR + d + 2] * w2;
+                        acr[r][3] += sq->xs[r * DTR + d + 3] * w3;
+                    }
+                }
+                float bv = a.qb[layer][n];
+#pragma unroll
+                for (int r = 0; r < ROWS; ++r)
+                    qkvb[(size_t)(m0 + r) * 480 + n] = bv + (acr[r][0] + acr[r][1]) + (acr[r][2] + acr[r][3]);
+            }
+        }
+        gridbar(bar, gen, 5 + layer * 4);
+
+        if (wb < 256) {
+            SAttn* sa = (SAttn*)smem;
+            int kq = wb & 7, bh = wb >> 3;
+            int b = bh >> 2, h = bh & 3;
+            int k0 = kq * KQLEN;
+            int k1 = min(LMAX, k0 + KQLEN);
+            int klen = max(k1 - k0, 0);
+            for (int i = tid; i < klen * DH; i += 256) {
+                int kk = i / DH, d = i - kk * DH;
+                size_t base = (size_t)(b * LMAX + k0 + kk) * 480;
+                sa->K[i] = qkvb[base + DTR + h * DH + d];
+                sa->V[i] = qkvb[base + 2 * DTR + h * DH + d];
+            }
+            __syncthreads();
+            int q = tid;
+            if (q < LMAX) {
+                float4 qv[10];
+                const float4* qr = (const float4*)(qkvb + (size_t)(b * LMAX + q) * 480 + h * DH);
+#pragma unroll
+                for (int i = 0; i < 10; ++i) qv[i] = qr[i];
+                int len = lens[b];
+                const float scale = 0.15811388300841898f;
+                float m = -INFINITY, l = 0.f;
+                float o[DH];
+#pragma unroll
+                for (int d = 0; d < DH; ++d) o[d] = 0.f;
+                int kend = min(k1, len);
+                for (int k = k0; k < kend; ++k) {
+                    const float4* kr = (const float4*)&sa->K[(k - k0) * DH];
+                    float s0 = 0.f, s1 = 0.f, s2 = 0.f, s3 = 0.f;
+#pragma unroll
+                    for (int i = 0; i < 10; ++i) {
+                        float4 kv = kr[i];
+                        s0 += qv[i].x * kv.x; s1 += qv[i].y * kv.y;
+                        s2 += qv[i].z * kv.z; s3 += qv[i].w * kv.w;
+                    }
+                    float s = ((s0 + s1) + (s2 + s3)) * scale;
+                    float p;
+                    if (s <= m) {
+                        p = expf(s - m);
+                    } else {
+                        float c = expf(m - s);
+#pragma unroll
+                        for (int d = 0; d < DH; ++d) o[d] *= c;
+                        l *= c;
+                        m = s;
+                        p = 1.0f;
+                    }
+                    l += p;
+                    const float* vr = &sa->V[(k - k0) * DH];
+#pragma unroll
+                    for (int d = 0; d < DH; ++d) o[d] += p * vr[d];
+                }
+                float* pp = part + ((size_t)(bh * KSPLIT + kq) * LMAX + q) * 42;
+#pragma unroll
+                for (int d = 0; d < DH; ++d) pp[d] = o[d];
+                pp[40] = l;
+                pp[41] = m;
+            }
+        }
+        gridbar(bar, gen, 6 + layer * 4);
+
+        {
+            SProj* sp = (SProj*)smem;
+            int m0 = wb * ROWS;
+            int g = tid >> 6, lane = tid & 63;
+            for (int pr = g; pr < ROWS * NHEADS; pr += 4) {
+                int r = pr >> 2, h = pr & 3;
+                int row = m0 + r;
+                int b = row / LMAX, q = row - b * LMAX;
+                const float* pb = part + ((size_t)((b * NHEADS + h) * KSPLIT) * LMAX + q) * 42;
+                const size_t st = (size_t)LMAX * 42;
+                float ms = -INFINITY;
+#pragma unroll
+                for (int i = 0; i < KSPLIT; ++i) ms = fmaxf(ms, pb[i * st + 41]);
+                float lsum = 0.f, acc = 0.f;
+#pragma unroll
+                for (int i = 0; i < KSPLIT; ++i) {
+                    float w = expf(pb[i * st + 41] - ms);
+                    lsum += w * pb[i * st + 40];
+                    if (lane < DH) acc += w * pb[i * st + lane];
+                }
+                if (lane < DH) sp->xs[r * DTR + h * DH + lane] = acc / lsum;
+            }
+            __syncthreads();
+            if (tid < DTR) {
+                int n = tid;
+                float acr[ROWS][4];
+#pragma unroll
+                for (int r = 0; r < ROWS; ++r) { acr[r][0] = acr[r][1] = acr[r][2] = acr[r][3] = 0.f; }
+                for (int d = 0; d < DTR; d += 4) {
+                    float w0 = outT[(size_t)(d + 0) * DTR + n];
+                    float w1 = outT[(size_t)(d + 1) * DTR + n];
+                    float w2 = outT[(size_t)(d + 2) * DTR + n];
+                    float w3 = outT[(size_t)(d + 3) * DTR + n];
+#pragma unroll
+                    for (int r = 0; r < ROWS; ++r) {
+                        acr[r][0] += sp->xs[r * DTR + d] * w0;
+                        acr[r][1] += sp->xs[r * DTR + d + 1] * w1;
+                        acr[r][2] += sp->xs[r * DTR + d + 2] * w2;
+                        acr[r][3] += sp->xs[r * DTR + d + 3] * w3;
+                    }
+                }
+                float bv = a.ob[layer][n];
+#pragma unroll
+                for (int r = 0; r < ROWS; ++r)
+                    sp->ys[r * DTR + n] = bv + (acr[r][0] + acr[r][1]) + (acr[r][2] + acr[r][3])
+                                          + in_x[(size_t)(m0 + r) * DTR + n];
+            }
+            __syncthreads();
+            if (g < ROWS)
+                wave_ln_row(&sp->ys[g * DTR], lane, a.l1w[layer], a.l1b[layer],
+                            x2 + (size_t)(m0 + g) * DTR);
+        }
+        gridbar(bar, gen, 7 + layer * 4);
+
+        {
+            SFf* sf = (SFf*)smem;
+            int m0 = wb * ROWS;
+            int last = (layer == 1);
+            for (int i = tid; i < ROWS * DTR; i += 256) sf->xs[i] = x2[(size_t)m0 * DTR + i];
+            __syncthreads();
+            {
+                int n = tid;
+                float acr[ROWS][4];
+#pragma unroll
+                for (int r = 0; r < ROWS; ++r) { acr[r][0] = acr[r][1] = acr[r][2] = acr[r][3] = 0.f; }
+                for (int d = 0; d < DTR; d += 4) {
+                    float w0 = ff1T[(size_t)(d + 0) * NHID2 + n];
+                    float w1 = ff1T[(size_t)(d + 1) * NHID2 + n];
+                    float w2 = ff1T[(size_t)(d + 2) * NHID2 + n];
+                    float w3 = ff1T[(size_t)(d + 3) * NHID2 + n];
+#pragma unroll
+                    for (int r = 0; r < ROWS; ++r) {
+                        acr[r][0] += sf->xs[r * DTR + d] * w0;
+                        acr[r][1] += sf->xs[r * DTR + d + 1] * w1;
+                        acr[r][2] += sf->xs[r * DTR + d + 2] * w2;
+                        acr[r][3] += sf->xs[r * DTR + d + 3] * w3;
+                    }
+                }
+                float bv = a.f1b[layer][n];
+#pragma unroll
+                for (int r = 0; r < ROWS; ++r)
+                    sf->hs[r * NHID2 + n] = fmaxf(bv + (acr[r][0] + acr[r][1]) + (acr[r][2] + acr[r][3]), 0.f);
+            }
+            __syncthreads();
+            if (tid < DTR) {
+                int n = tid;
+                float acr[ROWS][4];
+#pragma unroll
+                for (int r = 0; r < ROWS; ++r) { acr[r][0] = acr[r][1] = acr[r][2] = acr[r][3] = 0.f; }
+                for (int d = 0; d < NHID2; d += 4) {
+                    float w0 = ff2T[(size_t)(d + 0) * DTR + n];
+                    float w1 = ff2T[(size_t)(d + 1) * DTR + n];
+                    float w2 = ff2T[(size_t)(d + 2) * DTR + n];
+                    float w3 = ff2T[(size_t)(d + 3) * DTR + n];
+#pragma unroll
+                    for (int r = 0; r < ROWS; ++r) {
+                        acr[r][0] += sf->hs[r * NHID2 + d] * w0;
+                        acr[r][1] += sf->hs[r * NHID2 + d + 1] * w1;
+                        acr[r][2] += sf->hs[r * NHID2 + d + 2] * w2;
+                        acr[r][3] += sf->hs[r * NHID2 + d + 3] * w3;
+                    }
+                }
+                float bv = a.f2b[layer][n];
+#pragma unroll
+                for (int r = 0; r < ROWS; ++r)
+                    sf->zs[r * DTR + n] = bv + (acr[r][0] + acr[r][1]) + (acr[r][2] + acr[r][3]) + sf->xs[r * DTR + n];
+            }
+            __syncthreads();
+            int wid = tid >> 6, lane = tid & 63;
+            if (!last) {
+                if (wid < ROWS)
+                    wave_ln_row(&sf->zs[wid * DTR], lane, a.l2w[layer], a.l2b[layer],
+                                ff_out + (size_t)(m0 + wid) * DTR);
+            } else {
+                if (wid < ROWS)
+                    wave_ln_row(&sf->zs[wid * DTR], lane, a.l2w[layer], a.l2b[layer],
+                                &sf->fin[wid * DTR]);
+                __syncthreads();
+                for (int i = tid; i < ROWS * DTR; i += 256) ff_out[(size_t)m0 * DTR + i] = sf->fin[i];
+                int row = m0 + wid;
+                int b = row / LMAX, l = row - b * LMAX;
+                float np = (l < lens[b]) ? 1.f : 0.f;
+                if (lane < 37) {
+                    const float* w = (lane < 36) ? (a.wtype + lane * DTR) : a.wtime;
+                    const float* fr = &sf->fin[wid * DTR];
+                    float acc = 0.f;
+#pragma unroll 8
+                    for (int d = 0; d < DTR; d += 4) {
+                        float4 w4 = *(const float4*)(w + d);
+                        acc += fr[d] * w4.x + fr[d + 1] * w4.y + fr[d + 2] * w4.z + fr[d + 3] * w4.w;
+                    }
+                    acc *= np;
+                    if (lane < 36) ff_out[OUT_TYPE + (size_t)row * NND + lane] = acc;
+                    else ff_out[OUT_TIME + row] = acc;
+                }
+            }
+        }
+        if (layer == 0) gridbar(bar, gen, 8);
     }
 }
+
+extern "C" void kernel_launch(void* const* d_in, const int* in_sizes, int n_in,
+                              void* d_out, int out_size, void* d_ws, size_t ws_size,
+                              hipStream_t stream) {
+    MegaArgs a;
+    a.et    = (const int*)d_in[0];
+    a.etime = (const float*)d_in[1];
+    a.Ru    = (const float*)d_in[2];
+    a.gs    = (const float*)d_in[3];
+    a.Winc  = (const float*)d_in[4];
+    a.binc  = (const float*)d_in[5];
+    a.mapw  = (const float*)d_in[6];
+    a.wtime = (const float*)d_in[7];
+    a.wtype = (const float*)d_in[8];
+    for (int layer = 0; layer < 2; ++layer) {
+        int base = 9 + layer * 12;
+        a.qw[layer]  = (const float*)d_in[base + 0];
+        a.qb[layer]  = (const float*)d_in[base + 1];
+        a.ow[layer]  = (const float*)d_in[base + 2];
+        a.ob[layer]  = (const float*)d_in[base + 3];
+        a.f1w[layer] = (const float*)d_in[base + 4];
+        a.f1b[layer] = (const float*)d_in[base + 5];
+        a.f2w[layer] = (const float*)d_in[base + 6];
+        a.f2b[layer] = (const float*)d_in[base + 7];
+        a.l1w[layer] = (const float*)d_in[base + 8];
+        a.l1b[layer] = (const float*)d_in[base + 9];
+        a.l2w[layer] = (const float*)d_in[base + 10];
+        a.l2b[layer] = (const float*)d_in[base + 11];
+    }
+    a.ws   = (float*)d_ws;
+    a.outp = (float*)d_out;
+
+    k_mega<<<NBLK, 256, 0, stream>>>(a);
+}
```
